# Kernel optimization log

Hardware: AMD Instinct MI355X
Metric: run time of the kernel (lower is better)

The kernel has to match this reference:

```python
import jax, jax.numpy as jnp
import numpy as np

MAX_SEQ_LEN = 1000

def _ln(x, g, b, eps=1e-5):
    m = jnp.mean(x, -1, keepdims=True)
    v = jnp.var(x, -1, keepdims=True)
    return (x - m) * jax.lax.rsqrt(v + eps) * g + b

def _conv1d(x, k, b):
    # x [B,T,Cin], k [K,Cin,Cout], 'SAME' padding (odd kernel)
    return jax.lax.conv_general_dilated(x, k, (1,), 'SAME', dimension_numbers=('NWC', 'WIO', 'NWC')) + b

def _dwconv(x, w):
    # lightweight conv: softmax-normalized depthwise kernel, w [C,K]
    k = jnp.transpose(jax.nn.softmax(w, axis=1))[:, None, :]  # [K,1,C]
    return jax.lax.conv_general_dilated(x, k, (1,), 'SAME', dimension_numbers=('NWC', 'WIO', 'NWC'), feature_group_count=x.shape[-1])

def _conv2d(x, k, b):
    # x [B,H,W,Cin], k [kh,kw,Cin,Cout]
    return jax.lax.conv_general_dilated(x, k, (1, 1), 'SAME', dimension_numbers=('NHWC', 'HWIO', 'NHWC')) + b

def _lconv(x, mask, ln_g, ln_b, glu_w, glu_b, dw, out_w, out_b):
    # LConvBlock: LN -> GLU projection -> depthwise lightweight conv -> out proj -> residual, masked
    res = x
    h = _ln(x, ln_g, ln_b)
    h = h @ glu_w + glu_b
    a, g = jnp.split(h, 2, axis=-1)
    h = a * jax.nn.sigmoid(g)
    h = jnp.where(mask[..., None], 0.0, h)
    h = _dwconv(h, dw)
    h = h @ out_w + out_b
    h = h + res
    return jnp.where(mask[..., None], 0.0, h)

def _forward(content_embedding, speaker_embedding_B, rhythm_B, scaled_duration_outputs,
             in_w, in_b,
             lc0_ln_g, lc0_ln_b, lc0_glu_w, lc0_glu_b, lc0_dw, lc0_out_w, lc0_out_b,
             lc1_ln_g, lc1_ln_b, lc1_glu_w, lc1_glu_b, lc1_dw, lc1_out_w, lc1_out_b,
             p1_w, p1_b, p2_k, p2_b,
             cw_k, cw_b, cw_ln_g, cw_ln_b,
             mkb1_k, mkb1_b, mkb2_k, mkb2_b,
             lw_w, lw_b, ln_g, ln_b, text_mask):
    B, S, _ = content_embedding.shape
    spk = jnp.broadcast_to(speaker_embedding_B[:, None, :], (B, S, speaker_embedding_B.shape[-1]))
    x = jnp.concatenate([content_embedding, spk], -1) @ in_w + in_b
    # duration predictor
    V = _lconv(x, text_mask, lc0_ln_g, lc0_ln_b, lc0_glu_w, lc0_glu_b, lc0_dw, lc0_out_w, lc0_out_b)
    V = _lconv(V, text_mask, lc1_ln_g, lc1_ln_b, lc1_glu_w, lc1_glu_b, lc1_dw, lc1_out_w, lc1_out_b)
    D = jax.nn.softplus(V @ p1_w + p1_b)[..., 0]
    D = jnp.where(text_mask, 0.0, D)
    T = _conv1d(V, p2_k, p2_b)  # [B,S,upsampled_dim]
    # learnable upsampling
    pred_phoneme_len = scaled_duration_outputs.sum(-1)
    alpha_B = jax.lax.stop_gradient(pred_phoneme_len / rhythm_B) / D.sum(-1)
    sD = alpha_B[:, None] * D
    sV = alpha_B[:, None, None] * V
    sT = alpha_B[:, None, None] * T
    mel_len = jnp.clip(jnp.round(sD.sum(-1)).astype(jnp.int32), 1, MAX_SEQ_LEN)
    mel_mask = jnp.arange(MAX_SEQ_LEN)[None, :] >= mel_len[:, None]  # True = pad
    attn_mask = mel_mask[:, :, None] & text_mask[:, None, :]  # bmm(mel_mask, src_mask^T).bool()
    e_k = jnp.cumsum(sD, axis=1)
    s_k = e_k - sD
    t = jnp.arange(1, MAX_SEQ_LEN + 1, dtype=sD.dtype)[None, :, None]
    Sm = jnp.where(attn_mask, 0.0, t - s_k[:, None, :])
    Em = jnp.where(attn_mask, 0.0, e_k[:, None, :] - t)
    # conv_w block: conv1d -> relu -> LN
    Cv = _ln(jax.nn.relu(_conv1d(sV, cw_k, cw_b)), cw_ln_g, cw_ln_b)  # [B,S,CW]
    feat = jnp.concatenate([Sm[..., None], Em[..., None],
                            jnp.broadcast_to(Cv[:, None, :, :], (B, MAX_SEQ_LEN, S, Cv.shape[-1]))], -1)
    h = jax.nn.silu(_conv2d(feat, mkb1_k, mkb1_b))
    h = jax.nn.silu(_conv2d(h, mkb2_k, mkb2_b))
    Wsc = (h @ lw_w + lw_b)[..., 0]  # [B,mel,S]
    Wsc = jnp.where(attn_mask | text_mask[:, None, :], -jnp.inf, Wsc)
    Wmat = jax.nn.softmax(Wsc, axis=2)
    up = jnp.matmul(Wmat, sT)
    up = _ln(up, ln_g, ln_b)
    up = jnp.where(mel_mask[..., None], 0.0, up)
    return up, Wmat, alpha_B, mel_len, mel_mask

def setup_inputs() -> dict:
    key = jax.random.key(0)
    ks = iter(jax.random.split(key, 64))
    B, S, DC, DS, H, CW, MKB, K = 8, 256, 192, 64, 256, 16, 16, 3
    def w(shape, scale=0.02):
        return jax.random.normal(next(ks), shape, jnp.float32) * scale
    inp = {}
    inp['content_embedding'] = jax.random.normal(next(ks), (B, S, DC), jnp.float32)
    inp['speaker_embedding_B'] = jax.random.normal(next(ks), (B, DS), jnp.float32)
    inp['rhythm_B'] = 0.15 + 0.1 * jax.random.uniform(next(ks), (B,), jnp.float32)
    inp['scaled_duration_outputs'] = jax.random.uniform(next(ks), (B, S), jnp.float32)
    lens = jax.random.randint(next(ks), (B,), 200, S + 1)
    inp['text_mask'] = jnp.arange(S)[None, :] >= lens[:, None]
    inp['in_w'] = w((DC + DS, H)); inp['in_b'] = jnp.zeros((H,), jnp.float32)
    for i in range(2):
        inp[f'lc{i}_ln_g'] = jnp.ones((H,), jnp.float32); inp[f'lc{i}_ln_b'] = jnp.zeros((H,), jnp.float32)
        inp[f'lc{i}_glu_w'] = w((H, 2 * H)); inp[f'lc{i}_glu_b'] = jnp.zeros((2 * H,), jnp.float32)
        inp[f'lc{i}_dw'] = w((H, K), 1.0)
        inp[f'lc{i}_out_w'] = w((H, H)); inp[f'lc{i}_out_b'] = jnp.zeros((H,), jnp.float32)
    inp['p1_w'] = w((H, 1)); inp['p1_b'] = jnp.zeros((1,), jnp.float32)
    inp['p2_k'] = w((K, H, H)); inp['p2_b'] = jnp.zeros((H,), jnp.float32)
    inp['cw_k'] = w((K, H, CW)); inp['cw_b'] = jnp.zeros((CW,), jnp.float32)
    inp['cw_ln_g'] = jnp.ones((CW,), jnp.float32); inp['cw_ln_b'] = jnp.zeros((CW,), jnp.float32)
    inp['mkb1_k'] = w((K, K, CW + 2, MKB)); inp['mkb1_b'] = jnp.zeros((MKB,), jnp.float32)
    inp['mkb2_k'] = w((K, K, MKB, MKB)); inp['mkb2_b'] = jnp.zeros((MKB,), jnp.float32)
    inp['lw_w'] = w((MKB, 1)); inp['lw_b'] = jnp.zeros((1,), jnp.float32)
    inp['ln_g'] = jnp.ones((H,), jnp.float32); inp['ln_b'] = jnp.zeros((H,), jnp.float32)
    return inp

def reference(content_embedding, speaker_embedding_B, rhythm_B, scaled_duration_outputs,
              text_mask,
              in_w, in_b,
              lc0_ln_g, lc0_ln_b, lc0_glu_w, lc0_glu_b, lc0_dw, lc0_out_w, lc0_out_b,
              lc1_ln_g, lc1_ln_b, lc1_glu_w, lc1_glu_b, lc1_dw, lc1_out_w, lc1_out_b,
              p1_w, p1_b, p2_k, p2_b,
              cw_k, cw_b, cw_ln_g, cw_ln_b,
              mkb1_k, mkb1_b, mkb2_k, mkb2_b,
              lw_w, lw_b, ln_g, ln_b):
    return _forward(content_embedding, speaker_embedding_B, rhythm_B, scaled_duration_outputs,
                    in_w, in_b,
                    lc0_ln_g, lc0_ln_b, lc0_glu_w, lc0_glu_b, lc0_dw, lc0_out_w, lc0_out_b,
                    lc1_ln_g, lc1_ln_b, lc1_glu_w, lc1_glu_b, lc1_dw, lc1_out_w, lc1_out_b,
                    p1_w, p1_b, p2_k, p2_b,
                    cw_k, cw_b, cw_ln_g, cw_ln_b,
                    mkb1_k, mkb1_b, mkb2_k, mkb2_b,
                    lw_w, lw_b, ln_g, ln_b, text_mask)
```

## Files before the change

### kernel.cpp

```cpp
#include <hip/hip_runtime.h>
#include <math.h>

#define SS 256
#define HH 256
#define MLEN 1000
#define CWW 16
#define NOC 16
#define RB 24

typedef __attribute__((ext_vector_type(8))) short bfrag;
typedef __attribute__((ext_vector_type(4))) float ffrag;

#define WS_X      0u
#define WS_V1     524288u
#define WS_V2     1048576u
#define WS_HB     1572864u
#define WS_STT    1835008u
#define WS_WB     2097152u
#define WS_CCV    2424832u
#define WS_SSV    2457600u
#define WS_CCI    2490368u
#define WS_SSI    2523136u
#define WS_CP     2555904u
#define WS_CV     2654208u
#define WS_EK     2686976u
#define WS_SK     2689024u
#define WS_ALPHA  2691072u
#define WS_MELI   2691080u
#define WS_TMASK  2691088u

#define PK_IN     0u
#define PK_GLU0   65536u
#define PK_GLU1   196608u
#define PK_OUT0   327680u
#define PK_OUT1   393216u
#define PK_P2     458752u

#define OUT_UP    0u
#define OUT_W     2048000u
#define OUT_ALPHA 4096000u
#define OUT_MLEN  4096008u
#define OUT_MMASK 4096016u

__device__ __forceinline__ unsigned bf16rne(float x){
  unsigned u=__float_as_uint(x);
  u += 0x7fffu + ((u>>16)&1u);
  return u;
}
__device__ __forceinline__ unsigned short bf16h(float x){ return (unsigned short)(bf16rne(x)>>16); }
__device__ __forceinline__ float bf2f(unsigned short u){ return __uint_as_float(((unsigned)u)<<16); }
__device__ __forceinline__ unsigned frag_idx(int k,int n,int KT){
  return (unsigned)(((((n>>4)*KT+(k>>5))*64 + ((k>>3)&3)*16 + (n&15))<<3) + (k&7));
}

__global__ __launch_bounds__(256) void k_mask(const void* __restrict__ traw, float* __restrict__ ws){
  __shared__ int s_fu, s_ff, s_nz;
  const unsigned char* mb=(const unsigned char*)traw;
  const unsigned int*  mw=(const unsigned int*)traw;
  int tid=threadIdx.x;
  if(tid==0){s_fu=0;s_ff=0;s_nz=0;}
  __syncthreads();
  int fu=0,ff=0,nz=0;
  for(int w=tid;w<512;w+=256){
    unsigned int v=mw[w];
    if(v){ nz=1; if(v==0x3F800000u) ff=1; else if(v&0xFFFFFF00u) fu=1; }
  }
  if(fu) atomicOr(&s_fu,1);
  if(ff) atomicOr(&s_ff,1);
  if(nz) atomicOr(&s_nz,1);
  __syncthreads();
  int words = (s_ff || (!s_fu && s_nz));
  for(int i=tid;i<2048;i+=256){
    unsigned int v = words ? mw[i] : (unsigned int)mb[i];
    ws[WS_TMASK+i] = v ? 1.0f : 0.0f;
  }
}

__global__ __launch_bounds__(256) void k_prep(const float* __restrict__ in_w,
    const float* __restrict__ g0, const float* __restrict__ g1,
    const float* __restrict__ o0, const float* __restrict__ o1,
    const float* __restrict__ p2k, float* __restrict__ ws){
  unsigned short* wb=(unsigned short*)(ws+WS_WB);
  int gid=blockIdx.x*256+threadIdx.x, stride=gridDim.x*256;
  for(int i=gid;i<65536;i+=stride){ int k=i>>8,n=i&255; wb[PK_IN  +frag_idx(k,n,8)]=bf16h(in_w[i]); }
  for(int i=gid;i<131072;i+=stride){ int k=i>>9,n=i&511; wb[PK_GLU0+frag_idx(k,n,8)]=bf16h(g0[i]); }
  for(int i=gid;i<131072;i+=stride){ int k=i>>9,n=i&511; wb[PK_GLU1+frag_idx(k,n,8)]=bf16h(g1[i]); }
  for(int i=gid;i<65536;i+=stride){ int k=i>>8,n=i&255; wb[PK_OUT0+frag_idx(k,n,8)]=bf16h(o0[i]); }
  for(int i=gid;i<65536;i+=stride){ int k=i>>8,n=i&255; wb[PK_OUT1+frag_idx(k,n,8)]=bf16h(o1[i]); }
  for(int i=gid;i<196608;i+=stride){ int k3=i>>16,r=i&65535,k=r>>8,n=r&255;
    wb[PK_P2+(unsigned)k3*65536u+frag_idx(k,n,8)]=bf16h(p2k[i]); }
}

__global__ __launch_bounds__(256) void k_inproj2(const float* __restrict__ ce, const float* __restrict__ spk,
    const unsigned short* __restrict__ wb, const float* __restrict__ in_b, float* __restrict__ ws){
  __shared__ unsigned short Abf[16][264];
  int m0=(blockIdx.x>>1)*16, nh=blockIdx.x&1, tid=threadIdx.x, b=m0>>8;
  for(int it=0;it<16;it++){
    int m=m0+it;
    float v=(tid<192)? ce[m*192+tid] : spk[b*64+tid-192];
    Abf[it][tid]=bf16h(v);
  }
  __syncthreads();
  int w=tid>>6, lane=tid&63, lq=lane>>4, lm=lane&15;
  ffrag acc[2];
  #pragma unroll
  for(int tt=0;tt<2;tt++){ acc[tt][0]=0.f;acc[tt][1]=0.f;acc[tt][2]=0.f;acc[tt][3]=0.f; }
  #pragma unroll
  for(int kt=0;kt<8;kt++){
    bfrag af=*(const bfrag*)&Abf[lm][kt*32+lq*8];
    #pragma unroll
    for(int tt=0;tt<2;tt++){
      int nt=nh*8+w*2+tt;
      bfrag bf=*(const bfrag*)(wb+((((unsigned)(nt*8+kt))*64u+(unsigned)lane)<<3));
      acc[tt]=__builtin_amdgcn_mfma_f32_16x16x32_bf16(af,bf,acc[tt],0,0,0);
    }
  }
  #pragma unroll
  for(int tt=0;tt<2;tt++){
    int n=nh*128+w*32+tt*16+lm;
    float bn=in_b[n];
    #pragma unroll
    for(int reg=0;reg<4;reg++)
      ws[WS_X+(unsigned)(m0+lq*4+reg)*256u+n]=acc[tt][reg]+bn;
  }
}

__global__ __launch_bounds__(256) void k_glu2(const float* __restrict__ xin,
    const unsigned short* __restrict__ wb, const float* __restrict__ glu_b,
    const float* __restrict__ lgam, const float* __restrict__ lbet,
    const float* __restrict__ tmask, unsigned short* __restrict__ hout){
  __shared__ float Xf[16][264];
  __shared__ unsigned short Abf[16][264];
  __shared__ float gb[2][256];
  __shared__ float tmL[16];
  int m0=(blockIdx.x>>1)*16, nh=blockIdx.x&1, tid=threadIdx.x;
  gb[0][tid]=lgam[tid]; gb[1][tid]=lbet[tid];
  if(tid<16) tmL[tid]=tmask[m0+tid];
  for(int it=0;it<16;it++) Xf[it][tid]=xin[(unsigned)(m0+it)*256u+tid];
  __syncthreads();
  int r=tid>>4, seg=tid&15;
  float s=0.f,q=0.f;
  #pragma unroll
  for(int j4=0;j4<4;j4++){
    float4 v=*(const float4*)&Xf[r][seg*16+j4*4];
    s+=v.x+v.y+v.z+v.w; q+=v.x*v.x+v.y*v.y+v.z*v.z+v.w*v.w;
  }
  s+=__shfl_xor(s,1); q+=__shfl_xor(q,1);
  s+=__shfl_xor(s,2); q+=__shfl_xor(q,2);
  s+=__shfl_xor(s,4); q+=__shfl_xor(q,4);
  s+=__shfl_xor(s,8); q+=__shfl_xor(q,8);
  float mean=s*(1.0f/256.0f), rstd=rsqrtf(q*(1.0f/256.0f)-mean*mean+1e-5f);
  #pragma unroll
  for(int j4=0;j4<4;j4++){
    int c=seg*16+j4*4;
    float4 v=*(const float4*)&Xf[r][c];
    unsigned short o0=bf16h((v.x-mean)*rstd*gb[0][c+0]+gb[1][c+0]);
    unsigned short o1=bf16h((v.y-mean)*rstd*gb[0][c+1]+gb[1][c+1]);
    unsigned short o2=bf16h((v.z-mean)*rstd*gb[0][c+2]+gb[1][c+2]);
    unsigned short o3=bf16h((v.w-mean)*rstd*gb[0][c+3]+gb[1][c+3]);
    *(uint2*)&Abf[r][c]=make_uint2((unsigned)o0|((unsigned)o1<<16),(unsigned)o2|((unsigned)o3<<16));
  }
  __syncthreads();
  int w=tid>>6, lane=tid&63, lq=lane>>4, lm=lane&15;
  ffrag aca[2], acg[2];
  #pragma unroll
  for(int tt=0;tt<2;tt++){ aca[tt][0]=0;aca[tt][1]=0;aca[tt][2]=0;aca[tt][3]=0;
                           acg[tt][0]=0;acg[tt][1]=0;acg[tt][2]=0;acg[tt][3]=0; }
  #pragma unroll
  for(int kt=0;kt<8;kt++){
    bfrag af=*(const bfrag*)&Abf[lm][kt*32+lq*8];
    #pragma unroll
    for(int tt=0;tt<2;tt++){
      int nta=nh*8+w*2+tt, ntg=nta+16;
      bfrag bfa=*(const bfrag*)(wb+((((unsigned)(nta*8+kt))*64u+(unsigned)lane)<<3));
      bfrag bfg=*(const bfrag*)(wb+((((unsigned)(ntg*8+kt))*64u+(unsigned)lane)<<3));
      aca[tt]=__builtin_amdgcn_mfma_f32_16x16x32_bf16(af,bfa,aca[tt],0,0,0);
      acg[tt]=__builtin_amdgcn_mfma_f32_16x16x32_bf16(af,bfg,acg[tt],0,0,0);
    }
  }
  #pragma unroll
  for(int tt=0;tt<2;tt++){
    int n=nh*128+w*32+tt*16+lm;
    float ba=glu_b[n], bg=glu_b[n+256];
    #pragma unroll
    for(int reg=0;reg<4;reg++){
      int row=lq*4+reg;
      float a=aca[tt][reg]+ba, g=acg[tt][reg]+bg;
      float hv=a*(1.0f/(1.0f+__expf(-g)));
      if(tmL[row]!=0.0f) hv=0.0f;
      hout[(unsigned)(m0+row)*256u+n]=bf16h(hv);
    }
  }
}

__global__ __launch_bounds__(256) void k_dwout2(const unsigned short* __restrict__ hb,
    const float* __restrict__ resid, const unsigned short* __restrict__ wb,
    const float* __restrict__ dw, const float* __restrict__ out_b,
    const float* __restrict__ tmask, float* __restrict__ vout){
  __shared__ unsigned short Hb[18][264];
  __shared__ unsigned short Abf[16][264];
  __shared__ float dws[3][256];
  __shared__ float tmL[16];
  int m0=(blockIdx.x>>1)*16, nh=blockIdx.x&1, tid=threadIdx.x, b=m0>>8, s0=m0&255;
  for(int it=0;it<18;it++){
    int sI=s0-1+it;
    Hb[it][tid]=(sI>=0&&sI<256)? hb[(unsigned)(b*256+sI)*256u+tid] : (unsigned short)0;
  }
  {
    float d0=dw[tid*3],d1=dw[tid*3+1],d2=dw[tid*3+2];
    float mx=fmaxf(d0,fmaxf(d1,d2));
    float e0=expf(d0-mx),e1=expf(d1-mx),e2=expf(d2-mx);
    float inv=1.0f/(e0+e1+e2);
    dws[0][tid]=e0*inv; dws[1][tid]=e1*inv; dws[2][tid]=e2*inv;
  }
  if(tid<16) tmL[tid]=tmask[m0+tid];
  __syncthreads();
  float w0=dws[0][tid],w1=dws[1][tid],w2=dws[2][tid];
  for(int it=0;it<16;it++){
    float a=w0*bf2f(Hb[it][tid])+w1*bf2f(Hb[it+1][tid])+w2*bf2f(Hb[it+2][tid]);
    Abf[it][tid]=bf16h(a);
  }
  __syncthreads();
  int w=tid>>6, lane=tid&63, lq=lane>>4, lm=lane&15;
  ffrag acc[2];
  #pragma unroll
  for(int tt=0;tt<2;tt++){ acc[tt][0]=0;acc[tt][1]=0;acc[tt][2]=0;acc[tt][3]=0; }
  #pragma unroll
  for(int kt=0;kt<8;kt++){
    bfrag af=*(const bfrag*)&Abf[lm][kt*32+lq*8];
    #pragma unroll
    for(int tt=0;tt<2;tt++){
      int nt=nh*8+w*2+tt;
      bfrag bf=*(const bfrag*)(wb+((((unsigned)(nt*8+kt))*64u+(unsigned)lane)<<3));
      acc[tt]=__builtin_amdgcn_mfma_f32_16x16x32_bf16(af,bf,acc[tt],0,0,0);
    }
  }
  #pragma unroll
  for(int tt=0;tt<2;tt++){
    int n=nh*128+w*32+tt*16+lm;
    float bn=out_b[n];
    #pragma unroll
    for(int reg=0;reg<4;reg++){
      int row=lq*4+reg, m=m0+row;
      float v=acc[tt][reg]+bn+resid[(unsigned)m*256u+n];
      vout[(unsigned)m*256u+n]=(tmL[row]!=0.0f)?0.0f:v;
    }
  }
}

__global__ __launch_bounds__(256) void k_dur(const float* __restrict__ V2, const float* __restrict__ p1w,
    const float* __restrict__ p1b, const float* __restrict__ sdo, const float* __restrict__ rhythm,
    float* __restrict__ ws, float* __restrict__ outp){
  __shared__ float p1[HH];
  __shared__ float sd[SS];
  __shared__ float red[16];
  int b=blockIdx.x, tid=threadIdx.x;
  int wid=tid>>6, lane=tid&63;
  p1[tid]=p1w[tid];
  __syncthreads();
  float accd=p1b[0];
  const float* row=V2+(unsigned)(b*SS+tid)*HH;
  for(int k=0;k<HH;k+=4){
    float4 v=*(const float4*)&row[k];
    accd+=v.x*p1[k]+v.y*p1[k+1]+v.z*p1[k+2]+v.w*p1[k+3];
  }
  float Dv=fmaxf(accd,0.0f)+log1pf(expf(-fabsf(accd)));
  if(ws[WS_TMASK+b*SS+tid]!=0.0f) Dv=0.0f;
  float sv=sdo[b*SS+tid];
  float a=Dv, c=sv;
  for(int off=32;off;off>>=1){ a+=__shfl_down(a,off); c+=__shfl_down(c,off); }
  if(lane==0){ red[wid]=a; red[wid+8]=c; }
  __syncthreads();
  float Dsum=red[0]+red[1]+red[2]+red[3];
  float pred=red[8]+red[9]+red[10]+red[11];
  float al=(pred/rhythm[b])/Dsum;
  float sDv=al*Dv;
  sd[tid]=sDv;
  __syncthreads();
  for(int off=1;off<SS;off<<=1){
    float t=(tid>=off)?sd[tid-off]:0.0f;
    __syncthreads();
    sd[tid]+=t;
    __syncthreads();
  }
  float ek=sd[tid], sk=ek-sDv;
  ws[WS_EK+b*SS+tid]=ek;
  ws[WS_SK+b*SS+tid]=sk;
  float melf=sd[SS-1];
  int mel=(int)rintf(melf); mel=mel<1?1:(mel>MLEN?MLEN:mel);
  if(tid==0){
    ws[WS_ALPHA+b]=al;
    ((int*)ws)[WS_MELI+b]=mel;
    outp[OUT_ALPHA+b]=al;
    outp[OUT_MLEN+b]=(float)mel;
  }
  for(int t=tid;t<MLEN;t+=SS) outp[OUT_MMASK+b*MLEN+t]=(t>=mel)?1.0f:0.0f;
}

__global__ __launch_bounds__(256) void k_T2(const float* __restrict__ V2,
    const unsigned short* __restrict__ wb, const float* __restrict__ p2b, float* __restrict__ ws){
  __shared__ unsigned short Abf[18][264];
  int m0=(blockIdx.x>>1)*16, nh=blockIdx.x&1, tid=threadIdx.x, b=m0>>8, s0=m0&255;
  for(int it=0;it<18;it++){
    int sI=s0-1+it;
    float v=(sI>=0&&sI<256)? V2[(unsigned)(b*256+sI)*256u+tid] : 0.0f;
    Abf[it][tid]=bf16h(v);
  }
  __syncthreads();
  int w=tid>>6, lane=tid&63, lq=lane>>4, lm=lane&15;
  ffrag acc[2];
  #pragma unroll
  for(int tt=0;tt<2;tt++){ acc[tt][0]=0;acc[tt][1]=0;acc[tt][2]=0;acc[tt][3]=0; }
  for(int k3=0;k3<3;k3++){
    const unsigned short* wb3=wb+(unsigned)k3*65536u;
    #pragma unroll
    for(int kt=0;kt<8;kt++){
      bfrag af=*(const bfrag*)&Abf[lm+k3][kt*32+lq*8];
      #pragma unroll
      for(int tt=0;tt<2;tt++){
        int nt=nh*8+w*2+tt;
        bfrag bf=*(const bfrag*)(wb3+((((unsigned)(nt*8+kt))*64u+(unsigned)lane)<<3));
        acc[tt]=__builtin_amdgcn_mfma_f32_16x16x32_bf16(af,bf,acc[tt],0,0,0);
      }
    }
  }
  float al=ws[WS_ALPHA+b];
  unsigned short* stt=(unsigned short*)(ws+WS_STT);
  #pragma unroll
  for(int tt=0;tt<2;tt++){
    int n=nh*128+w*32+tt*16+lm;
    float bn=p2b[n];
    unsigned short o0=bf16h((acc[tt][0]+bn)*al);
    unsigned short o1=bf16h((acc[tt][1]+bn)*al);
    unsigned short o2=bf16h((acc[tt][2]+bn)*al);
    unsigned short o3=bf16h((acc[tt][3]+bn)*al);
    *(uint2*)&stt[((unsigned)(b*256+n)<<8)+(unsigned)(s0+lq*4)]=
      make_uint2((unsigned)o0|((unsigned)o1<<16),(unsigned)o2|((unsigned)o3<<16));
  }
}

__global__ __launch_bounds__(256) void k_cv(const float* __restrict__ V2, const float* __restrict__ cwk,
    const float* __restrict__ cwb, const float* __restrict__ cwg, const float* __restrict__ cwbe,
    float* __restrict__ ws){
  __shared__ float Vt[18][SS];
  int b=blockIdx.x>>4, tile=blockIdx.x&15, tid=threadIdx.x;
  int sbase=tile*16;
  float al=ws[WS_ALPHA+b];
  for(int rr=0;rr<18;rr++){
    int s=sbase-1+rr;
    Vt[rr][tid]=(s>=0&&s<SS)?al*V2[(b*SS+s)*HH+tid]:0.0f;
  }
  __syncthreads();
  int sl=tid>>4, oc=tid&15;
  float a0=cwb[oc],a1=0.f,a2=0.f,a3=0.f;
  for(int k3=0;k3<3;k3++){
    const float* vp=&Vt[sl+k3][0];
    const float* wpp=cwk+(unsigned)k3*HH*CWW+oc;
    for(int c=0;c<HH;c+=4){
      a0+=vp[c+0]*wpp[(c+0)*CWW];
      a1+=vp[c+1]*wpp[(c+1)*CWW];
      a2+=vp[c+2]*wpp[(c+2)*CWW];
      a3+=vp[c+3]*wpp[(c+3)*CWW];
    }
  }
  float acc=fmaxf((a0+a1)+(a2+a3),0.0f);
  float ssum=acc, qsum=acc*acc;
  for(int off=8;off;off>>=1){ ssum+=__shfl_xor(ssum,off); qsum+=__shfl_xor(qsum,off); }
  float mean=ssum*(1.0f/CWW), var=qsum*(1.0f/CWW)-mean*mean;
  float cv=(acc-mean)*rsqrtf(var+1e-5f)*cwg[oc]+cwbe[oc];
  ws[WS_CV+(unsigned)(b*SS+sbase+sl)*CWW+oc]=cv;
}

__global__ __launch_bounds__(256) void k_cp(const float* __restrict__ mkb1k, const float* __restrict__ mkb1b,
    float* __restrict__ ws){
  __shared__ float CvL[258][17];
  __shared__ float k1c[3][3][CWW][NOC];
  __shared__ float kab[3][3][2][NOC];
  __shared__ float skE[258], ekE[258], fiE[258];
  int b=blockIdx.x, tid=threadIdx.x;
  for(int i=tid;i<3*3*CWW*NOC;i+=256){
    int oc=i&15, ic=(i>>4)&15, kk=i>>8;
    int kw=kk%3, kh=kk/3;
    k1c[kh][kw][ic][oc]=mkb1k[((kh*3+kw)*18+2+ic)*NOC+oc];
  }
  for(int i=tid;i<3*3*2*NOC;i+=256){
    int oc=i&15, ch=(i>>4)&1, kk=i>>5;
    int kw=kk%3, kh=kk/3;
    kab[kh][kw][ch][oc]=mkb1k[((kh*3+kw)*18+ch)*NOC+oc];
  }
  for(int i=tid;i<SS*CWW;i+=256) CvL[1+(i>>4)][i&15]=ws[WS_CV+(unsigned)b*SS*CWW+i];
  if(tid<CWW){ CvL[0][tid]=0.f; CvL[257][tid]=0.f; }
  if(tid<258){
    float sk=0.f, ek=0.f, fi=0.f;
    if(tid>=1 && tid<=SS){
      sk=ws[WS_SK+b*SS+tid-1];
      ek=ws[WS_EK+b*SS+tid-1];
      fi=(ws[WS_TMASK+b*SS+tid-1]!=0.0f)?0.0f:1.0f;
    }
    skE[tid]=sk; ekE[tid]=ek; fiE[tid]=fi;
  }
  __syncthreads();
  float* cpg=ws+WS_CP+(unsigned)b*3*SS*NOC;
  float ccv[16],ssv[16],cci[16],ssi[16];
  #pragma unroll
  for(int oc=0;oc<NOC;oc++){ float bb=mkb1b[oc]; ccv[oc]=bb; cci[oc]=bb; ssv[oc]=0.f; ssi[oc]=0.f; }
  for(int dt=0;dt<3;dt++){
    float acc[NOC];
    #pragma unroll
    for(int oc=0;oc<NOC;oc++) acc[oc]=0.f;
    #pragma unroll
    for(int ds=0;ds<3;ds++){
      #pragma unroll
      for(int ic=0;ic<CWW;ic++){
        float v=CvL[tid+ds][ic];
        #pragma unroll
        for(int oc=0;oc<NOC;oc++) acc[oc]+=v*k1c[dt][ds][ic][oc];
      }
    }
    for(int oc=0;oc<NOC;oc++) cpg[(unsigned)(dt*SS+tid)*NOC+oc]=acc[oc];
    float va[16],vb[16],ia[16],ib2[16];
    #pragma unroll
    for(int oc=0;oc<NOC;oc++){ va[oc]=0.f; vb[oc]=0.f; ia[oc]=0.f; ib2[oc]=0.f; }
    #pragma unroll
    for(int ds=0;ds<3;ds++){
      int j=tid+ds;
      float inb=(j>=1&&j<=SS)?1.0f:0.0f;
      float fb=fiE[j];
      float skv=skE[j], ekv=ekE[j];
      #pragma unroll
      for(int oc=0;oc<NOC;oc++){
        float ka=kab[dt][ds][0][oc], kb=kab[dt][ds][1][oc];
        float d=ka-kb, e=kb*ekv-ka*skv;
        va[oc]+=inb*d; vb[oc]+=inb*e; ia[oc]+=fb*d; ib2[oc]+=fb*e;
      }
    }
    float dtf=(float)dt;
    #pragma unroll
    for(int oc=0;oc<NOC;oc++){
      ccv[oc]+=acc[oc]+vb[oc]+dtf*va[oc]; ssv[oc]+=va[oc];
      cci[oc]+=acc[oc]+ib2[oc]+dtf*ia[oc]; ssi[oc]+=ia[oc];
    }
  }
  unsigned base=(unsigned)(b*SS+tid)*16u;
  for(int oc=0;oc<NOC;oc++){
    ws[WS_CCV+base+oc]=ccv[oc];
    ws[WS_SSV+base+oc]=ssv[oc];
    ws[WS_CCI+base+oc]=cci[oc];
    ws[WS_SSI+base+oc]=ssi[oc];
  }
}

__global__ __launch_bounds__(256,3) void k_stageB(
    const float* __restrict__ ws, const float* __restrict__ mkb1k, const float* __restrict__ mkb1b,
    const float* __restrict__ mkb2k, const float* __restrict__ mkb2b,
    const float* __restrict__ lww, const float* __restrict__ lwb,
    float* __restrict__ outp){
  __shared__ short ringh[3][258][RB];
  __shared__ float skL[258], ekL[258], finL[258];
  __shared__ float wscL[SS];
  __shared__ float red[16];
  int bx=blockIdx.x, b=bx/125, chunk=bx%125, t0=chunk*8, tid=threadIdx.x;
  int wid=tid>>6, lane=tid&63;
  int lq=lane>>4, lm=lane&15;
  if(tid<258){
    float sk=0.f, ek=0.f, fin=0.f;
    if(tid>=1 && tid<=SS){
      sk=ws[WS_SK+b*SS+tid-1];
      ek=ws[WS_EK+b*SS+tid-1];
      fin=(ws[WS_TMASK+b*SS+tid-1]!=0.0f)?0.0f:1.0f;
    }
    skL[tid]=sk; ekL[tid]=ek; finL[tid]=fin;
  }
  if(tid<72){
    int sl=tid/24, rem=tid%24;
    int row=(rem<12)?0:257, c=(rem%12)*2;
    *(int*)&ringh[sl][row][c]=0;
  }
  int mel=((const int*)ws)[WS_MELI+b];
  __syncthreads();

  const float* cpb=ws+WS_CP+(unsigned)b*3*SS*NOC;

  unsigned offA[5]; int dtL[5], zgL[5];
  bfrag bfw[5];
  {
    #pragma unroll
    for(int i=0;i<5;i++){
      int g=4*i+lq;
      int dt,ds,hf,zg;
      if(g<18){ dt=g/6; int rm=g-6*dt; ds=rm>>1; hf=rm&1; zg=0; }
      else { dt=0; ds=0; hf=0; zg=1; }
      int srow=wid*64+lm+ds;
      offA[i]=(unsigned)((srow*RB+8*hf)*2);
      dtL[i]=dt; zgL[i]=zg;
      int pk[4];
      if(!zg){
        #pragma unroll
        for(int j=0;j<4;j++){
          unsigned u0=bf16rne(mkb2k[(8*g+2*j)*NOC+lm]);
          unsigned u1=bf16rne(mkb2k[(8*g+2*j+1)*NOC+lm]);
          pk[j]=(int)((u0>>16)|(u1&0xffff0000u));
        }
      } else pk[0]=pk[1]=pk[2]=pk[3]=0;
      bfw[i]=__builtin_bit_cast(bfrag, make_int4(pk[0],pk[1],pk[2],pk[3]));
    }
  }
  float b2v=mkb2b[lm];
  float lwwv=lww[lm];
  float lwb0=lwb[0];
  const char* ringB=(const char*)&ringh[0][0][0];
  bfrag azero={};

  auto conv1row=[&](int T){
    int s=tid;
    float acc[NOC];
    bool fv=(T>=1)&&(T<=998)&&(T+1<mel);
    bool fi=(T>=2)&&(T<=998)&&(T-1>=mel);
    if(fv||fi){
      const float* cc=ws+(fv?WS_CCV:WS_CCI)+(unsigned)(b*SS+s)*16u;
      const float* s2=ws+(fv?WS_SSV:WS_SSI)+(unsigned)(b*SS+s)*16u;
      float Tf=(float)T;
      #pragma unroll
      for(int q=0;q<4;q++){
        float4 c4=((const float4*)cc)[q];
        float4 s4=((const float4*)s2)[q];
        acc[4*q+0]=c4.x+Tf*s4.x; acc[4*q+1]=c4.y+Tf*s4.y;
        acc[4*q+2]=c4.z+Tf*s4.z; acc[4*q+3]=c4.w+Tf*s4.w;
      }
    } else {
      #pragma unroll
      for(int oc=0;oc<NOC;oc++) acc[oc]=mkb1b[oc];
      #pragma unroll
      for(int dt=0;dt<3;dt++){
        int tr=T+dt-1;
        if(tr<0||tr>=MLEN) continue;
        bool valid=(tr<mel);
        float tt=(float)(tr+1);
        float gg[3], hh[3];
        #pragma unroll
        for(int ds=0;ds<3;ds++){
          int j=s+ds;
          float f = valid ? ((j>=1&&j<=SS)?1.0f:0.0f) : finL[j];
          gg[ds]=f*(tt-skL[j]);
          hh[ds]=f*(ekL[j]-tt);
        }
        const float* cpr=cpb+(unsigned)(dt*SS+s)*NOC;
        float4 c0=((const float4*)cpr)[0], c1=((const float4*)cpr)[1];
        float4 c2=((const float4*)cpr)[2], c3=((const float4*)cpr)[3];
        acc[0]+=c0.x; acc[1]+=c0.y; acc[2]+=c0.z; acc[3]+=c0.w;
        acc[4]+=c1.x; acc[5]+=c1.y; acc[6]+=c1.z; acc[7]+=c1.w;
        acc[8]+=c2.x; acc[9]+=c2.y; acc[10]+=c2.z; acc[11]+=c2.w;
        acc[12]+=c3.x; acc[13]+=c3.y; acc[14]+=c3.z; acc[15]+=c3.w;
        #pragma unroll
        for(int ds=0;ds<3;ds++){
          const float* kA=mkb1k+((dt*3+ds)*18+0)*NOC;
          const float* kB=mkb1k+((dt*3+ds)*18+1)*NOC;
          #pragma unroll
          for(int oc=0;oc<NOC;oc++) acc[oc]+=gg[ds]*kA[oc]+hh[ds]*kB[oc];
        }
      }
    }
    int slot=T%3;
    int pk[8];
    #pragma unroll
    for(int j=0;j<8;j++){
      float x0=acc[2*j], x1=acc[2*j+1];
      float s0=x0/(1.0f+__expf(-x0));
      float s1=x1/(1.0f+__expf(-x1));
      unsigned u0=bf16rne(s0), u1=bf16rne(s1);
      pk[j]=(int)((u0>>16)|(u1&0xffff0000u));
    }
    int4* dst=(int4*)&ringh[slot][s+1][0];
    dst[0]=make_int4(pk[0],pk[1],pk[2],pk[3]);
    dst[1]=make_int4(pk[4],pk[5],pk[6],pk[7]);
  };

  if(t0>0) conv1row(t0-1);
  conv1row(t0);

  #pragma unroll 1
  for(int r=0;r<8;r++){
    int t=t0+r;
    if(t+1<MLEN) conv1row(t+1);
    __syncthreads();
    int tmod=t%3;
    ffrag acc2[4];
    #pragma unroll
    for(int tt=0;tt<4;tt++){ acc2[tt][0]=b2v; acc2[tt][1]=b2v; acc2[tt][2]=b2v; acc2[tt][3]=b2v; }
    #pragma unroll
    for(int i=0;i<5;i++){
      int dt=dtL[i];
      int x=tmod+dt+2; x=(x>=3)?x-3:x; x=(x>=3)?x-3:x;
      int tr=t+dt-1;
      bool av=((unsigned)tr<(unsigned)MLEN)&&(!zgL[i]);
      const char* rp=ringB+(unsigned)x*(258u*RB*2u)+offA[i];
      #pragma unroll
      for(int tt=0;tt<4;tt++){
        int4 ra=*(const int4*)(rp+tt*(16*RB*2));
        bfrag a=av?__builtin_bit_cast(bfrag,ra):azero;
        acc2[tt]=__builtin_amdgcn_mfma_f32_16x16x32_bf16(a,bfw[i],acc2[tt],0,0,0);
      }
    }
    #pragma unroll
    for(int tt=0;tt<4;tt++){
      float out4[4];
      #pragma unroll
      for(int q=0;q<4;q++){
        float xx=acc2[tt][q];
        float pv=(xx/(1.0f+__expf(-xx)))*lwwv;
        pv+=__shfl_xor(pv,1); pv+=__shfl_xor(pv,2); pv+=__shfl_xor(pv,4); pv+=__shfl_xor(pv,8);
        out4[q]=pv+lwb0;
      }
      if(lm==0){
        *(float4*)&wscL[wid*64+tt*16+lq*4]=make_float4(out4[0],out4[1],out4[2],out4[3]);
      }
    }
    __syncthreads();
    float fm=finL[tid+1];
    float wsc=wscL[tid];
    float val=(fm!=0.0f)?wsc:-3.0e38f;
    float mx=val;
    for(int off=32;off;off>>=1) mx=fmaxf(mx,__shfl_down(mx,off));
    if(lane==0) red[wid]=mx;
    __syncthreads();
    mx=fmaxf(fmaxf(red[0],red[1]),fmaxf(red[2],red[3]));
    float e=(fm!=0.0f)?__expf(wsc-mx):0.0f;
    float sm=e;
    for(int off=32;off;off>>=1) sm+=__shfl_down(sm,off);
    if(lane==0) red[8+wid]=sm;
    __syncthreads();
    sm=red[8]+red[9]+red[10]+red[11];
    outp[OUT_W+(unsigned)(b*MLEN+t)*SS+tid]=e/sm;
    __syncthreads();
  }
}

__global__ __launch_bounds__(256) void k_up(const float* __restrict__ ws,
    const float* __restrict__ lng, const float* __restrict__ lnb, float* __restrict__ outp){
  __shared__ unsigned short Wbf[16][264];
  __shared__ float UpL[16][264];
  __shared__ float gb[2][256];
  int bx=blockIdx.x, b=bx/63, tile=bx%63, t0=tile*16, tid=threadIdx.x;
  gb[0][tid]=lng[tid]; gb[1][tid]=lnb[tid];
  for(int it=0;it<16;it++){
    int t=t0+it;
    float v=(t<MLEN)? outp[OUT_W+(unsigned)(b*MLEN+t)*256u+tid] : 0.0f;
    Wbf[it][tid]=bf16h(v);
  }
  int mel=((const int*)ws)[WS_MELI+b];
  __syncthreads();
  int w=tid>>6, lane=tid&63, lq=lane>>4, lm=lane&15;
  const unsigned short* stt=(const unsigned short*)(ws+WS_STT)+(unsigned)b*65536u;
  ffrag acc[4];
  #pragma unroll
  for(int tt=0;tt<4;tt++){ acc[tt][0]=0;acc[tt][1]=0;acc[tt][2]=0;acc[tt][3]=0; }
  #pragma unroll
  for(int kt=0;kt<8;kt++){
    bfrag af=*(const bfrag*)&Wbf[lm][kt*32+lq*8];
    #pragma unroll
    for(int tt=0;tt<4;tt++){
      int n=w*64+tt*16+lm;
      bfrag bf=*(const bfrag*)(stt+((unsigned)n<<8)+(unsigned)(kt*32+lq*8));
      acc[tt]=__builtin_amdgcn_mfma_f32_16x16x32_bf16(af,bf,acc[tt],0,0,0);
    }
  }
  #pragma unroll
  for(int tt=0;tt<4;tt++){
    #pragma unroll
    for(int reg=0;reg<4;reg++)
      UpL[lq*4+reg][w*64+tt*16+lm]=acc[tt][reg];
  }
  __syncthreads();
  int r=tid>>4, seg=tid&15;
  float s=0.f,q=0.f;
  #pragma unroll
  for(int j4=0;j4<4;j4++){
    float4 v=*(const float4*)&UpL[r][seg*16+j4*4];
    s+=v.x+v.y+v.z+v.w; q+=v.x*v.x+v.y*v.y+v.z*v.z+v.w*v.w;
  }
  s+=__shfl_xor(s,1); q+=__shfl_xor(q,1);
  s+=__shfl_xor(s,2); q+=__shfl_xor(q,2);
  s+=__shfl_xor(s,4); q+=__shfl_xor(q,4);
  s+=__shfl_xor(s,8); q+=__shfl_xor(q,8);
  float mean=s*(1.0f/256.0f), rstd=rsqrtf(q*(1.0f/256.0f)-mean*mean+1e-5f);
  int t=t0+r;
  if(t<MLEN){
    bool vld=(t<mel);
    #pragma unroll
    for(int j4=0;j4<4;j4++){
      int c=seg*16+j4*4;
      float4 v=*(const float4*)&UpL[r][c];
      float4 o;
      o.x=vld?((v.x-mean)*rstd*gb[0][c+0]+gb[1][c+0]):0.0f;
      o.y=vld?((v.y-mean)*rstd*gb[0][c+1]+gb[1][c+1]):0.0f;
      o.z=vld?((v.z-mean)*rstd*gb[0][c+2]+gb[1][c+2]):0.0f;
      o.w=vld?((v.w-mean)*rstd*gb[0][c+3]+gb[1][c+3]):0.0f;
      *(float4*)&outp[OUT_UP+(unsigned)(b*MLEN+t)*256u+c]=o;
    }
  }
}

extern "C" void kernel_launch(void* const* d_in, const int* in_sizes, int n_in,
                              void* d_out, int out_size, void* d_ws, size_t ws_size,
                              hipStream_t stream){
  const float* ce   =(const float*)d_in[0];
  const float* spk  =(const float*)d_in[1];
  const float* rhy  =(const float*)d_in[2];
  const float* sdo  =(const float*)d_in[3];
  const void*  tmr  =d_in[4];
  const float* in_w =(const float*)d_in[5];
  const float* in_b =(const float*)d_in[6];
  const float* l0lg =(const float*)d_in[7];
  const float* l0lb =(const float*)d_in[8];
  const float* l0gw =(const float*)d_in[9];
  const float* l0gb =(const float*)d_in[10];
  const float* l0dw =(const float*)d_in[11];
  const float* l0ow =(const float*)d_in[12];
  const float* l0ob =(const float*)d_in[13];
  const float* l1lg =(const float*)d_in[14];
  const float* l1lb =(const float*)d_in[15];
  const float* l1gw =(const float*)d_in[16];
  const float* l1gb =(const float*)d_in[17];
  const float* l1dw =(const float*)d_in[18];
  const float* l1ow =(const float*)d_in[19];
  const float* l1ob =(const float*)d_in[20];
  const float* p1w  =(const float*)d_in[21];
  const float* p1b  =(const float*)d_in[22];
  const float* p2k  =(const float*)d_in[23];
  const float* p2b  =(const float*)d_in[24];
  const float* cwk  =(const float*)d_in[25];
  const float* cwb  =(const float*)d_in[26];
  const float* cwg  =(const float*)d_in[27];
  const float* cwbe =(const float*)d_in[28];
  const float* m1k  =(const float*)d_in[29];
  const float* m1b  =(const float*)d_in[30];
  const float* m2k  =(const float*)d_in[31];
  const float* m2b  =(const float*)d_in[32];
  const float* lww  =(const float*)d_in[33];
  const float* lwbp =(const float*)d_in[34];
  const float* lng  =(const float*)d_in[35];
  const float* lnb  =(const float*)d_in[36];
  float* ws=(float*)d_ws;
  float* outp=(float*)d_out;
  const unsigned short* wbb=(const unsigned short*)(ws+WS_WB);
  unsigned short* hb=(unsigned short*)(ws+WS_HB);

  k_mask   <<<1,256,0,stream>>>(tmr, ws);
  k_prep   <<<256,256,0,stream>>>(in_w, l0gw, l1gw, l0ow, l1ow, p2k, ws);
  k_inproj2<<<256,256,0,stream>>>(ce, spk, wbb+PK_IN, in_b, ws);
  k_glu2   <<<256,256,0,stream>>>(ws+WS_X,  wbb+PK_GLU0, l0gb, l0lg, l0lb, ws+WS_TMASK, hb);
  k_dwout2 <<<256,256,0,stream>>>(hb, ws+WS_X,  wbb+PK_OUT0, l0dw, l0ob, ws+WS_TMASK, ws+WS_V1);
  k_glu2   <<<256,256,0,stream>>>(ws+WS_V1, wbb+PK_GLU1, l1gb, l1lg, l1lb, ws+WS_TMASK, hb);
  k_dwout2 <<<256,256,0,stream>>>(hb, ws+WS_V1, wbb+PK_OUT1, l1dw, l1ob, ws+WS_TMASK, ws+WS_V2);
  k_dur    <<<8,256,0,stream>>>(ws+WS_V2, p1w, p1b, sdo, rhy, ws, outp);
  k_T2     <<<256,256,0,stream>>>(ws+WS_V2, wbb+PK_P2, p2b, ws);
  k_cv     <<<128,256,0,stream>>>(ws+WS_V2, cwk, cwb, cwg, cwbe, ws);
  k_cp     <<<8,256,0,stream>>>(m1k, m1b, ws);
  k_stageB <<<1000,256,0,stream>>>(ws, m1k, m1b, m2k, m2b, lww, lwbp, outp);
  k_up     <<<504,256,0,stream>>>(ws, lng, lnb, outp);
}
```

Before: 328.2 us.

## Fuse front-end LConv pipeline into one halo-tiled kernel and merge post kernels

Merges the mask and weight-prep kernels into one launch. The in-projection, both LConv blocks (LN, GLU, depthwise conv, out-projection, residual) now run in a single kernel per 8-row tile, recomputing a halo of neighbouring rows so intermediates stay in shared memory instead of going through global workspace. T2, cv and cp are folded into one post kernel. stageB stores its mask as bytes and raises the occupancy hint. The aim is fewer launches and less global traffic, paid for with redundant halo rows (8 useful of 16 MFMA rows) and more shared memory per block.

```diff
diff --git a/kernel.cpp b/kernel.cpp
--- a/kernel.cpp
+++ b/kernel.cpp
@@ -11,10 +11,7 @@
 typedef __attribute__((ext_vector_type(8))) short bfrag;
 typedef __attribute__((ext_vector_type(4))) float ffrag;
 
-#define WS_X      0u
-#define WS_V1     524288u
 #define WS_V2     1048576u
-#define WS_HB     1572864u
 #define WS_STT    1835008u
 #define WS_WB     2097152u
 #define WS_CCV    2424832u
@@ -53,35 +50,36 @@
   return (unsigned)(((((n>>4)*KT+(k>>5))*64 + ((k>>3)&3)*16 + (n&15))<<3) + (k&7));
 }
 
-__global__ __launch_bounds__(256) void k_mask(const void* __restrict__ traw, float* __restrict__ ws){
-  __shared__ int s_fu, s_ff, s_nz;
-  const unsigned char* mb=(const unsigned char*)traw;
-  const unsigned int*  mw=(const unsigned int*)traw;
-  int tid=threadIdx.x;
-  if(tid==0){s_fu=0;s_ff=0;s_nz=0;}
-  __syncthreads();
-  int fu=0,ff=0,nz=0;
-  for(int w=tid;w<512;w+=256){
-    unsigned int v=mw[w];
-    if(v){ nz=1; if(v==0x3F800000u) ff=1; else if(v&0xFFFFFF00u) fu=1; }
-  }
-  if(fu) atomicOr(&s_fu,1);
-  if(ff) atomicOr(&s_ff,1);
-  if(nz) atomicOr(&s_nz,1);
-  __syncthreads();
-  int words = (s_ff || (!s_fu && s_nz));
-  for(int i=tid;i<2048;i+=256){
-    unsigned int v = words ? mw[i] : (unsigned int)mb[i];
-    ws[WS_TMASK+i] = v ? 1.0f : 0.0f;
-  }
-}
-
-__global__ __launch_bounds__(256) void k_prep(const float* __restrict__ in_w,
+__global__ __launch_bounds__(256) void k_prepmask(const void* __restrict__ traw,
+    const float* __restrict__ in_w,
     const float* __restrict__ g0, const float* __restrict__ g1,
     const float* __restrict__ o0, const float* __restrict__ o1,
     const float* __restrict__ p2k, float* __restrict__ ws){
+  int tid=threadIdx.x;
+  if(blockIdx.x==256){
+    __shared__ int s_fu, s_ff, s_nz;
+    const unsigned char* mb=(const unsigned char*)traw;
+    const unsigned int*  mw=(const unsigned int*)traw;
+    if(tid==0){s_fu=0;s_ff=0;s_nz=0;}
+    __syncthreads();
+    int fu=0,ff=0,nz=0;
+    for(int w=tid;w<512;w+=256){
+      unsigned int v=mw[w];
+      if(v){ nz=1; if(v==0x3F800000u) ff=1; else if(v&0xFFFFFF00u) fu=1; }
+    }
+    if(fu) atomicOr(&s_fu,1);
+    if(ff) atomicOr(&s_ff,1);
+    if(nz) atomicOr(&s_nz,1);
+    __syncthreads();
+    int words = (s_ff || (!s_fu && s_nz));
+    for(int i=tid;i<2048;i+=256){
+      unsigned int v = words ? mw[i] : (unsigned int)mb[i];
+      ws[WS_TMASK+i] = v ? 1.0f : 0.0f;
+    }
+    return;
+  }
   unsigned short* wb=(unsigned short*)(ws+WS_WB);
-  int gid=blockIdx.x*256+threadIdx.x, stride=gridDim.x*256;
+  int gid=blockIdx.x*256+tid, stride=65536;
   for(int i=gid;i<65536;i+=stride){ int k=i>>8,n=i&255; wb[PK_IN  +frag_idx(k,n,8)]=bf16h(in_w[i]); }
   for(int i=gid;i<131072;i+=stride){ int k=i>>9,n=i&511; wb[PK_GLU0+frag_idx(k,n,8)]=bf16h(g0[i]); }
   for(int i=gid;i<131072;i+=stride){ int k=i>>9,n=i&511; wb[PK_GLU1+frag_idx(k,n,8)]=bf16h(g1[i]); }
@@ -91,159 +89,268 @@
     wb[PK_P2+(unsigned)k3*65536u+frag_idx(k,n,8)]=bf16h(p2k[i]); }
 }
 
-__global__ __launch_bounds__(256) void k_inproj2(const float* __restrict__ ce, const float* __restrict__ spk,
-    const unsigned short* __restrict__ wb, const float* __restrict__ in_b, float* __restrict__ ws){
+__global__ __launch_bounds__(256) void k_front(
+    const float* __restrict__ ce, const float* __restrict__ spk,
+    const unsigned short* __restrict__ wb, const float* __restrict__ in_b,
+    const float* __restrict__ g0b, const float* __restrict__ ln0g, const float* __restrict__ ln0b,
+    const float* __restrict__ dw0, const float* __restrict__ o0b,
+    const float* __restrict__ g1b, const float* __restrict__ ln1g, const float* __restrict__ ln1b,
+    const float* __restrict__ dw1, const float* __restrict__ o1b,
+    const float* __restrict__ tmask, float* __restrict__ V2){
   __shared__ unsigned short Abf[16][264];
-  int m0=(blockIdx.x>>1)*16, nh=blockIdx.x&1, tid=threadIdx.x, b=m0>>8;
+  __shared__ unsigned short Hb[16][264];
+  __shared__ float Xf[16][264];
+  __shared__ float Vf[16][264];
+  __shared__ float dws[2][3][256];
+  __shared__ float tmL[20];
+  int b=blockIdx.x>>5, tile=blockIdx.x&31, s0=tile*8, tid=threadIdx.x;
+  int w=tid>>6, lane=tid&63, lq=lane>>4, lm=lane&15;
+  {
+    float d0=dw0[tid*3],d1=dw0[tid*3+1],d2=dw0[tid*3+2];
+    float mx=fmaxf(d0,fmaxf(d1,d2));
+    float e0=__expf(d0-mx),e1=__expf(d1-mx),e2=__expf(d2-mx);
+    float inv=1.0f/(e0+e1+e2);
+    dws[0][0][tid]=e0*inv; dws[0][1][tid]=e1*inv; dws[0][2][tid]=e2*inv;
+    d0=dw1[tid*3];d1=dw1[tid*3+1];d2=dw1[tid*3+2];
+    mx=fmaxf(d0,fmaxf(d1,d2));
+    e0=__expf(d0-mx);e1=__expf(d1-mx);e2=__expf(d2-mx);
+    inv=1.0f/(e0+e1+e2);
+    dws[1][0][tid]=e0*inv; dws[1][1][tid]=e1*inv; dws[1][2][tid]=e2*inv;
+  }
+  if(tid<18){
+    int sI=s0-2+tid;
+    tmL[tid]=(sI>=0&&sI<256)? tmask[b*256+sI] : 1.0f;
+  }
   for(int it=0;it<16;it++){
-    int m=m0+it;
-    float v=(tid<192)? ce[m*192+tid] : spk[b*64+tid-192];
+    float v=0.f;
+    int sI=s0-2+it;
+    if(it<12 && sI>=0 && sI<256){
+      int m=b*256+sI;
+      v=(tid<192)? ce[m*192+tid] : spk[b*64+tid-192];
+    }
     Abf[it][tid]=bf16h(v);
   }
   __syncthreads();
-  int w=tid>>6, lane=tid&63, lq=lane>>4, lm=lane&15;
-  ffrag acc[2];
-  #pragma unroll
-  for(int tt=0;tt<2;tt++){ acc[tt][0]=0.f;acc[tt][1]=0.f;acc[tt][2]=0.f;acc[tt][3]=0.f; }
-  #pragma unroll
-  for(int kt=0;kt<8;kt++){
-    bfrag af=*(const bfrag*)&Abf[lm][kt*32+lq*8];
-    #pragma unroll
-    for(int tt=0;tt<2;tt++){
-      int nt=nh*8+w*2+tt;
-      bfrag bf=*(const bfrag*)(wb+((((unsigned)(nt*8+kt))*64u+(unsigned)lane)<<3));
-      acc[tt]=__builtin_amdgcn_mfma_f32_16x16x32_bf16(af,bf,acc[tt],0,0,0);
-    }
-  }
-  #pragma unroll
-  for(int tt=0;tt<2;tt++){
-    int n=nh*128+w*32+tt*16+lm;
-    float bn=in_b[n];
-    #pragma unroll
-    for(int reg=0;reg<4;reg++)
-      ws[WS_X+(unsigned)(m0+lq*4+reg)*256u+n]=acc[tt][reg]+bn;
-  }
-}
-
-__global__ __launch_bounds__(256) void k_glu2(const float* __restrict__ xin,
-    const unsigned short* __restrict__ wb, const float* __restrict__ glu_b,
-    const float* __restrict__ lgam, const float* __restrict__ lbet,
-    const float* __restrict__ tmask, unsigned short* __restrict__ hout){
-  __shared__ float Xf[16][264];
-  __shared__ unsigned short Abf[16][264];
-  __shared__ float gb[2][256];
-  __shared__ float tmL[16];
-  int m0=(blockIdx.x>>1)*16, nh=blockIdx.x&1, tid=threadIdx.x;
-  gb[0][tid]=lgam[tid]; gb[1][tid]=lbet[tid];
-  if(tid<16) tmL[tid]=tmask[m0+tid];
-  for(int it=0;it<16;it++) Xf[it][tid]=xin[(unsigned)(m0+it)*256u+tid];
-  __syncthreads();
-  int r=tid>>4, seg=tid&15;
-  float s=0.f,q=0.f;
-  #pragma unroll
-  for(int j4=0;j4<4;j4++){
-    float4 v=*(const float4*)&Xf[r][seg*16+j4*4];
-    s+=v.x+v.y+v.z+v.w; q+=v.x*v.x+v.y*v.y+v.z*v.z+v.w*v.w;
-  }
-  s+=__shfl_xor(s,1); q+=__shfl_xor(q,1);
-  s+=__shfl_xor(s,2); q+=__shfl_xor(q,2);
-  s+=__shfl_xor(s,4); q+=__shfl_xor(q,4);
-  s+=__shfl_xor(s,8); q+=__shfl_xor(q,8);
-  float mean=s*(1.0f/256.0f), rstd=rsqrtf(q*(1.0f/256.0f)-mean*mean+1e-5f);
-  #pragma unroll
-  for(int j4=0;j4<4;j4++){
-    int c=seg*16+j4*4;
-    float4 v=*(const float4*)&Xf[r][c];
-    unsigned short o0=bf16h((v.x-mean)*rstd*gb[0][c+0]+gb[1][c+0]);
-    unsigned short o1=bf16h((v.y-mean)*rstd*gb[0][c+1]+gb[1][c+1]);
-    unsigned short o2=bf16h((v.z-mean)*rstd*gb[0][c+2]+gb[1][c+2]);
-    unsigned short o3=bf16h((v.w-mean)*rstd*gb[0][c+3]+gb[1][c+3]);
-    *(uint2*)&Abf[r][c]=make_uint2((unsigned)o0|((unsigned)o1<<16),(unsigned)o2|((unsigned)o3<<16));
-  }
-  __syncthreads();
-  int w=tid>>6, lane=tid&63, lq=lane>>4, lm=lane&15;
-  ffrag aca[2], acg[2];
-  #pragma unroll
-  for(int tt=0;tt<2;tt++){ aca[tt][0]=0;aca[tt][1]=0;aca[tt][2]=0;aca[tt][3]=0;
-                           acg[tt][0]=0;acg[tt][1]=0;acg[tt][2]=0;acg[tt][3]=0; }
-  #pragma unroll
-  for(int kt=0;kt<8;kt++){
-    bfrag af=*(const bfrag*)&Abf[lm][kt*32+lq*8];
-    #pragma unroll
-    for(int tt=0;tt<2;tt++){
-      int nta=nh*8+w*2+tt, ntg=nta+16;
-      bfrag bfa=*(const bfrag*)(wb+((((unsigned)(nta*8+kt))*64u+(unsigned)lane)<<3));
-      bfrag bfg=*(const bfrag*)(wb+((((unsigned)(ntg*8+kt))*64u+(unsigned)lane)<<3));
-      aca[tt]=__builtin_amdgcn_mfma_f32_16x16x32_bf16(af,bfa,aca[tt],0,0,0);
-      acg[tt]=__builtin_amdgcn_mfma_f32_16x16x32_bf16(af,bfg,acg[tt],0,0,0);
-    }
-  }
-  #pragma unroll
-  for(int tt=0;tt<2;tt++){
-    int n=nh*128+w*32+tt*16+lm;
-    float ba=glu_b[n], bg=glu_b[n+256];
-    #pragma unroll
-    for(int reg=0;reg<4;reg++){
-      int row=lq*4+reg;
-      float a=aca[tt][reg]+ba, g=acg[tt][reg]+bg;
-      float hv=a*(1.0f/(1.0f+__expf(-g)));
-      if(tmL[row]!=0.0f) hv=0.0f;
-      hout[(unsigned)(m0+row)*256u+n]=bf16h(hv);
-    }
-  }
-}
-
-__global__ __launch_bounds__(256) void k_dwout2(const unsigned short* __restrict__ hb,
-    const float* __restrict__ resid, const unsigned short* __restrict__ wb,
-    const float* __restrict__ dw, const float* __restrict__ out_b,
-    const float* __restrict__ tmask, float* __restrict__ vout){
-  __shared__ unsigned short Hb[18][264];
-  __shared__ unsigned short Abf[16][264];
-  __shared__ float dws[3][256];
-  __shared__ float tmL[16];
-  int m0=(blockIdx.x>>1)*16, nh=blockIdx.x&1, tid=threadIdx.x, b=m0>>8, s0=m0&255;
-  for(int it=0;it<18;it++){
-    int sI=s0-1+it;
-    Hb[it][tid]=(sI>=0&&sI<256)? hb[(unsigned)(b*256+sI)*256u+tid] : (unsigned short)0;
-  }
-  {
-    float d0=dw[tid*3],d1=dw[tid*3+1],d2=dw[tid*3+2];
-    float mx=fmaxf(d0,fmaxf(d1,d2));
-    float e0=expf(d0-mx),e1=expf(d1-mx),e2=expf(d2-mx);
-    float inv=1.0f/(e0+e1+e2);
-    dws[0][tid]=e0*inv; dws[1][tid]=e1*inv; dws[2][tid]=e2*inv;
-  }
-  if(tid<16) tmL[tid]=tmask[m0+tid];
-  __syncthreads();
-  float w0=dws[0][tid],w1=dws[1][tid],w2=dws[2][tid];
-  for(int it=0;it<16;it++){
-    float a=w0*bf2f(Hb[it][tid])+w1*bf2f(Hb[it+1][tid])+w2*bf2f(Hb[it+2][tid]);
-    Abf[it][tid]=bf16h(a);
-  }
-  __syncthreads();
-  int w=tid>>6, lane=tid&63, lq=lane>>4, lm=lane&15;
-  ffrag acc[2];
-  #pragma unroll
-  for(int tt=0;tt<2;tt++){ acc[tt][0]=0;acc[tt][1]=0;acc[tt][2]=0;acc[tt][3]=0; }
-  #pragma unroll
-  for(int kt=0;kt<8;kt++){
-    bfrag af=*(const bfrag*)&Abf[lm][kt*32+lq*8];
-    #pragma unroll
-    for(int tt=0;tt<2;tt++){
-      int nt=nh*8+w*2+tt;
-      bfrag bf=*(const bfrag*)(wb+((((unsigned)(nt*8+kt))*64u+(unsigned)lane)<<3));
-      acc[tt]=__builtin_amdgcn_mfma_f32_16x16x32_bf16(af,bf,acc[tt],0,0,0);
-    }
-  }
-  #pragma unroll
-  for(int tt=0;tt<2;tt++){
-    int n=nh*128+w*32+tt*16+lm;
-    float bn=out_b[n];
-    #pragma unroll
-    for(int reg=0;reg<4;reg++){
-      int row=lq*4+reg, m=m0+row;
-      float v=acc[tt][reg]+bn+resid[(unsigned)m*256u+n];
-      vout[(unsigned)m*256u+n]=(tmL[row]!=0.0f)?0.0f:v;
+  {
+    ffrag acc[4];
+    #pragma unroll
+    for(int j=0;j<4;j++){acc[j][0]=0;acc[j][1]=0;acc[j][2]=0;acc[j][3]=0;}
+    #pragma unroll
+    for(int kt=0;kt<8;kt++){
+      bfrag af=*(const bfrag*)&Abf[lm][kt*32+lq*8];
+      #pragma unroll
+      for(int j=0;j<4;j++){
+        int nt=w*4+j;
+        bfrag bf=*(const bfrag*)(wb+PK_IN+((((unsigned)(nt*8+kt))*64u+(unsigned)lane)<<3));
+        acc[j]=__builtin_amdgcn_mfma_f32_16x16x32_bf16(af,bf,acc[j],0,0,0);
+      }
+    }
+    #pragma unroll
+    for(int j=0;j<4;j++){
+      int n=w*64+j*16+lm;
+      float bn=in_b[n];
+      #pragma unroll
+      for(int reg=0;reg<4;reg++) Xf[lq*4+reg][n]=acc[j][reg]+bn;
+    }
+  }
+  __syncthreads();
+  {
+    int r=tid>>4, seg=tid&15;
+    if(r<12){
+      float s=0.f,q=0.f;
+      #pragma unroll
+      for(int j4=0;j4<4;j4++){
+        float4 v=*(const float4*)&Xf[r][seg*16+j4*4];
+        s+=v.x+v.y+v.z+v.w; q+=v.x*v.x+v.y*v.y+v.z*v.z+v.w*v.w;
+      }
+      s+=__shfl_xor(s,1); q+=__shfl_xor(q,1);
+      s+=__shfl_xor(s,2); q+=__shfl_xor(q,2);
+      s+=__shfl_xor(s,4); q+=__shfl_xor(q,4);
+      s+=__shfl_xor(s,8); q+=__shfl_xor(q,8);
+      float mean=s*(1.0f/256.0f), rstd=rsqrtf(q*(1.0f/256.0f)-mean*mean+1e-5f);
+      #pragma unroll
+      for(int j4=0;j4<4;j4++){
+        int c=seg*16+j4*4;
+        float4 v=*(const float4*)&Xf[r][c];
+        unsigned short q0=bf16h((v.x-mean)*rstd*ln0g[c+0]+ln0b[c+0]);
+        unsigned short q1=bf16h((v.y-mean)*rstd*ln0g[c+1]+ln0b[c+1]);
+        unsigned short q2=bf16h((v.z-mean)*rstd*ln0g[c+2]+ln0b[c+2]);
+        unsigned short q3=bf16h((v.w-mean)*rstd*ln0g[c+3]+ln0b[c+3]);
+        *(uint2*)&Abf[r][c]=make_uint2((unsigned)q0|((unsigned)q1<<16),(unsigned)q2|((unsigned)q3<<16));
+      }
+    } else {
+      #pragma unroll
+      for(int j4=0;j4<4;j4++) *(uint2*)&Abf[r][seg*16+j4*4]=make_uint2(0,0);
+    }
+  }
+  __syncthreads();
+  {
+    ffrag aa[4],ag[4];
+    #pragma unroll
+    for(int j=0;j<4;j++){aa[j][0]=0;aa[j][1]=0;aa[j][2]=0;aa[j][3]=0;
+                         ag[j][0]=0;ag[j][1]=0;ag[j][2]=0;ag[j][3]=0;}
+    #pragma unroll
+    for(int kt=0;kt<8;kt++){
+      bfrag af=*(const bfrag*)&Abf[lm][kt*32+lq*8];
+      #pragma unroll
+      for(int j=0;j<4;j++){
+        int nta=w*4+j, ntg=nta+16;
+        bfrag bfa=*(const bfrag*)(wb+PK_GLU0+((((unsigned)(nta*8+kt))*64u+(unsigned)lane)<<3));
+        bfrag bfg=*(const bfrag*)(wb+PK_GLU0+((((unsigned)(ntg*8+kt))*64u+(unsigned)lane)<<3));
+        aa[j]=__builtin_amdgcn_mfma_f32_16x16x32_bf16(af,bfa,aa[j],0,0,0);
+        ag[j]=__builtin_amdgcn_mfma_f32_16x16x32_bf16(af,bfg,ag[j],0,0,0);
+      }
+    }
+    __syncthreads();
+    #pragma unroll
+    for(int j=0;j<4;j++){
+      int n=w*64+j*16+lm;
+      float ba=g0b[n], bg=g0b[n+256];
+      #pragma unroll
+      for(int reg=0;reg<4;reg++){
+        int row=lq*4+reg;
+        float a=aa[j][reg]+ba, g=ag[j][reg]+bg;
+        float hv=a*(1.0f/(1.0f+__expf(-g)));
+        if(row>=12||tmL[row]!=0.0f) hv=0.0f;
+        Hb[row][n]=bf16h(hv);
+      }
+    }
+  }
+  __syncthreads();
+  {
+    float w0=dws[0][0][tid],w1=dws[0][1][tid],w2=dws[0][2][tid];
+    for(int r=0;r<10;r++){
+      float a=w0*bf2f(Hb[r][tid])+w1*bf2f(Hb[r+1][tid])+w2*bf2f(Hb[r+2][tid]);
+      Abf[r][tid]=bf16h(a);
+    }
+    for(int r=10;r<16;r++) Abf[r][tid]=0;
+  }
+  __syncthreads();
+  {
+    ffrag acc[4];
+    #pragma unroll
+    for(int j=0;j<4;j++){acc[j][0]=0;acc[j][1]=0;acc[j][2]=0;acc[j][3]=0;}
+    #pragma unroll
+    for(int kt=0;kt<8;kt++){
+      bfrag af=*(const bfrag*)&Abf[lm][kt*32+lq*8];
+      #pragma unroll
+      for(int j=0;j<4;j++){
+        int nt=w*4+j;
+        bfrag bf=*(const bfrag*)(wb+PK_OUT0+((((unsigned)(nt*8+kt))*64u+(unsigned)lane)<<3));
+        acc[j]=__builtin_amdgcn_mfma_f32_16x16x32_bf16(af,bf,acc[j],0,0,0);
+      }
+    }
+    #pragma unroll
+    for(int j=0;j<4;j++){
+      int n=w*64+j*16+lm;
+      float bn=o0b[n];
+      #pragma unroll
+      for(int reg=0;reg<4;reg++){
+        int row=lq*4+reg;
+        float v=(row<10 && tmL[row+1]==0.0f)? acc[j][reg]+bn+Xf[row+1][n] : 0.0f;
+        Vf[row][n]=v;
+      }
+    }
+  }
+  __syncthreads();
+  {
+    int r=tid>>4, seg=tid&15;
+    if(r<10){
+      float s=0.f,q=0.f;
+      #pragma unroll
+      for(int j4=0;j4<4;j4++){
+        float4 v=*(const float4*)&Vf[r][seg*16+j4*4];
+        s+=v.x+v.y+v.z+v.w; q+=v.x*v.x+v.y*v.y+v.z*v.z+v.w*v.w;
+      }
+      s+=__shfl_xor(s,1); q+=__shfl_xor(q,1);
+      s+=__shfl_xor(s,2); q+=__shfl_xor(q,2);
+      s+=__shfl_xor(s,4); q+=__shfl_xor(q,4);
+      s+=__shfl_xor(s,8); q+=__shfl_xor(q,8);
+      float mean=s*(1.0f/256.0f), rstd=rsqrtf(q*(1.0f/256.0f)-mean*mean+1e-5f);
+      #pragma unroll
+      for(int j4=0;j4<4;j4++){
+        int c=seg*16+j4*4;
+        float4 v=*(const float4*)&Vf[r][c];
+        unsigned short q0=bf16h((v.x-mean)*rstd*ln1g[c+0]+ln1b[c+0]);
+        unsigned short q1=bf16h((v.y-mean)*rstd*ln1g[c+1]+ln1b[c+1]);
+        unsigned short q2=bf16h((v.z-mean)*rstd*ln1g[c+2]+ln1b[c+2]);
+        unsigned short q3=bf16h((v.w-mean)*rstd*ln1g[c+3]+ln1b[c+3]);
+        *(uint2*)&Abf[r][c]=make_uint2((unsigned)q0|((unsigned)q1<<16),(unsigned)q2|((unsigned)q3<<16));
+      }
+    } else {
+      #pragma unroll
+      for(int j4=0;j4<4;j4++) *(uint2*)&Abf[r][seg*16+j4*4]=make_uint2(0,0);
+    }
+  }
+  __syncthreads();
+  {
+    ffrag aa[4],ag[4];
+    #pragma unroll
+    for(int j=0;j<4;j++){aa[j][0]=0;aa[j][1]=0;aa[j][2]=0;aa[j][3]=0;
+                         ag[j][0]=0;ag[j][1]=0;ag[j][2]=0;ag[j][3]=0;}
+    #pragma unroll
+    for(int kt=0;kt<8;kt++){
+      bfrag af=*(const bfrag*)&Abf[lm][kt*32+lq*8];
+      #pragma unroll
+      for(int j=0;j<4;j++){
+        int nta=w*4+j, ntg=nta+16;
+        bfrag bfa=*(const bfrag*)(wb+PK_GLU1+((((unsigned)(nta*8+kt))*64u+(unsigned)lane)<<3));
+        bfrag bfg=*(const bfrag*)(wb+PK_GLU1+((((unsigned)(ntg*8+kt))*64u+(unsigned)lane)<<3));
+        aa[j]=__builtin_amdgcn_mfma_f32_16x16x32_bf16(af,bfa,aa[j],0,0,0);
+        ag[j]=__builtin_amdgcn_mfma_f32_16x16x32_bf16(af,bfg,ag[j],0,0,0);
+      }
+    }
+    __syncthreads();
+    #pragma unroll
+    for(int j=0;j<4;j++){
+      int n=w*64+j*16+lm;
+      float ba=g1b[n], bg=g1b[n+256];
+      #pragma unroll
+      for(int reg=0;reg<4;reg++){
+        int row=lq*4+reg;
+        float a=aa[j][reg]+ba, g=ag[j][reg]+bg;
+        float hv=a*(1.0f/(1.0f+__expf(-g)));
+        if(row>=10||tmL[row+1]!=0.0f) hv=0.0f;
+        Hb[row][n]=bf16h(hv);
+      }
+    }
+  }
+  __syncthreads();
+  {
+    float w0=dws[1][0][tid],w1=dws[1][1][tid],w2=dws[1][2][tid];
+    for(int r=0;r<8;r++){
+      float a=w0*bf2f(Hb[r][tid])+w1*bf2f(Hb[r+1][tid])+w2*bf2f(Hb[r+2][tid]);
+      Abf[r][tid]=bf16h(a);
+    }
+    for(int r=8;r<16;r++) Abf[r][tid]=0;
+  }
+  __syncthreads();
+  {
+    ffrag acc[4];
+    #pragma unroll
+    for(int j=0;j<4;j++){acc[j][0]=0;acc[j][1]=0;acc[j][2]=0;acc[j][3]=0;}
+    #pragma unroll
+    for(int kt=0;kt<8;kt++){
+      bfrag af=*(const bfrag*)&Abf[lm][kt*32+lq*8];
+      #pragma unroll
+      for(int j=0;j<4;j++){
+        int nt=w*4+j;
+        bfrag bf=*(const bfrag*)(wb+PK_OUT1+((((unsigned)(nt*8+kt))*64u+(unsigned)lane)<<3));
+        acc[j]=__builtin_amdgcn_mfma_f32_16x16x32_bf16(af,bf,acc[j],0,0,0);
+      }
+    }
+    #pragma unroll
+    for(int j=0;j<4;j++){
+      int n=w*64+j*16+lm;
+      float bn=o1b[n];
+      #pragma unroll
+      for(int reg=0;reg<4;reg++){
+        int row=lq*4+reg;
+        if(row<8){
+          float v=(tmL[row+2]!=0.0f)? 0.0f : acc[j][reg]+bn+Vf[row+1][n];
+          V2[(unsigned)(b*256+s0+row)*256u+n]=v;
+        }
+      }
     }
   }
 }
@@ -297,179 +404,181 @@
   for(int t=tid;t<MLEN;t+=SS) outp[OUT_MMASK+b*MLEN+t]=(t>=mel)?1.0f:0.0f;
 }
 
-__global__ __launch_bounds__(256) void k_T2(const float* __restrict__ V2,
-    const unsigned short* __restrict__ wb, const float* __restrict__ p2b, float* __restrict__ ws){
-  __shared__ unsigned short Abf[18][264];
-  int m0=(blockIdx.x>>1)*16, nh=blockIdx.x&1, tid=threadIdx.x, b=m0>>8, s0=m0&255;
-  for(int it=0;it<18;it++){
-    int sI=s0-1+it;
-    float v=(sI>=0&&sI<256)? V2[(unsigned)(b*256+sI)*256u+tid] : 0.0f;
-    Abf[it][tid]=bf16h(v);
-  }
-  __syncthreads();
-  int w=tid>>6, lane=tid&63, lq=lane>>4, lm=lane&15;
-  ffrag acc[2];
-  #pragma unroll
-  for(int tt=0;tt<2;tt++){ acc[tt][0]=0;acc[tt][1]=0;acc[tt][2]=0;acc[tt][3]=0; }
-  for(int k3=0;k3<3;k3++){
-    const unsigned short* wb3=wb+(unsigned)k3*65536u;
-    #pragma unroll
-    for(int kt=0;kt<8;kt++){
-      bfrag af=*(const bfrag*)&Abf[lm+k3][kt*32+lq*8];
-      #pragma unroll
-      for(int tt=0;tt<2;tt++){
-        int nt=nh*8+w*2+tt;
-        bfrag bf=*(const bfrag*)(wb3+((((unsigned)(nt*8+kt))*64u+(unsigned)lane)<<3));
-        acc[tt]=__builtin_amdgcn_mfma_f32_16x16x32_bf16(af,bf,acc[tt],0,0,0);
-      }
-    }
-  }
-  float al=ws[WS_ALPHA+b];
-  unsigned short* stt=(unsigned short*)(ws+WS_STT);
-  #pragma unroll
-  for(int tt=0;tt<2;tt++){
-    int n=nh*128+w*32+tt*16+lm;
-    float bn=p2b[n];
-    unsigned short o0=bf16h((acc[tt][0]+bn)*al);
-    unsigned short o1=bf16h((acc[tt][1]+bn)*al);
-    unsigned short o2=bf16h((acc[tt][2]+bn)*al);
-    unsigned short o3=bf16h((acc[tt][3]+bn)*al);
-    *(uint2*)&stt[((unsigned)(b*256+n)<<8)+(unsigned)(s0+lq*4)]=
-      make_uint2((unsigned)o0|((unsigned)o1<<16),(unsigned)o2|((unsigned)o3<<16));
+__global__ __launch_bounds__(256) void k_post(const float* __restrict__ V2,
+    const unsigned short* __restrict__ wbp2, const float* __restrict__ p2b,
+    const float* __restrict__ cwk, const float* __restrict__ cwb,
+    const float* __restrict__ cwg, const float* __restrict__ cwbe,
+    const float* __restrict__ mkb1k, const float* __restrict__ mkb1b,
+    float* __restrict__ ws){
+  int bx=blockIdx.x, tid=threadIdx.x;
+  if(bx<256){
+    __shared__ unsigned short Abf[18][264];
+    int m0=(bx>>1)*16, nh=bx&1, b=m0>>8, s0=m0&255;
+    for(int it=0;it<18;it++){
+      int sI=s0-1+it;
+      float v=(sI>=0&&sI<256)? V2[(unsigned)(b*256+sI)*256u+tid] : 0.0f;
+      Abf[it][tid]=bf16h(v);
+    }
+    __syncthreads();
+    int w=tid>>6, lane=tid&63, lq=lane>>4, lm=lane&15;
+    ffrag acc[2];
+    #pragma unroll
+    for(int tt=0;tt<2;tt++){ acc[tt][0]=0;acc[tt][1]=0;acc[tt][2]=0;acc[tt][3]=0; }
+    for(int k3=0;k3<3;k3++){
+      const unsigned short* wb3=wbp2+(unsigned)k3*65536u;
+      #pragma unroll
+      for(int kt=0;kt<8;kt++){
+        bfrag af=*(const bfrag*)&Abf[lm+k3][kt*32+lq*8];
+        #pragma unroll
+        for(int tt=0;tt<2;tt++){
+          int nt=nh*8+w*2+tt;
+          bfrag bf=*(const bfrag*)(wb3+((((unsigned)(nt*8+kt))*64u+(unsigned)lane)<<3));
+          acc[tt]=__builtin_amdgcn_mfma_f32_16x16x32_bf16(af,bf,acc[tt],0,0,0);
+        }
+      }
+    }
+    float al=ws[WS_ALPHA+b];
+    unsigned short* stt=(unsigned short*)(ws+WS_STT);
+    #pragma unroll
+    for(int tt=0;tt<2;tt++){
+      int n=nh*128+w*32+tt*16+lm;
+      float bn=p2b[n];
+      unsigned short o0=bf16h((acc[tt][0]+bn)*al);
+      unsigned short o1=bf16h((acc[tt][1]+bn)*al);
+      unsigned short o2=bf16h((acc[tt][2]+bn)*al);
+      unsigned short o3=bf16h((acc[tt][3]+bn)*al);
+      *(uint2*)&stt[((unsigned)(b*256+n)<<8)+(unsigned)(s0+lq*4)]=
+        make_uint2((unsigned)o0|((unsigned)o1<<16),(unsigned)o2|((unsigned)o3<<16));
+    }
+  } else if(bx<384){
+    __shared__ float Vt[18][SS];
+    int bb=bx-256;
+    int b=bb>>4, tile=bb&15;
+    int sbase=tile*16;
+    float al=ws[WS_ALPHA+b];
+    for(int rr=0;rr<18;rr++){
+      int s=sbase-1+rr;
+      Vt[rr][tid]=(s>=0&&s<SS)?al*V2[(b*SS+s)*HH+tid]:0.0f;
+    }
+    __syncthreads();
+    int sl=tid>>4, oc=tid&15;
+    float a0=cwb[oc],a1=0.f,a2=0.f,a3=0.f;
+    for(int k3=0;k3<3;k3++){
+      const float* vp=&Vt[sl+k3][0];
+      const float* wpp=cwk+(unsigned)k3*HH*CWW+oc;
+      for(int c=0;c<HH;c+=4){
+        a0+=vp[c+0]*wpp[(c+0)*CWW];
+        a1+=vp[c+1]*wpp[(c+1)*CWW];
+        a2+=vp[c+2]*wpp[(c+2)*CWW];
+        a3+=vp[c+3]*wpp[(c+3)*CWW];
+      }
+    }
+    float acc=fmaxf((a0+a1)+(a2+a3),0.0f);
+    float ssum=acc, qsum=acc*acc;
+    for(int off=8;off;off>>=1){ ssum+=__shfl_xor(ssum,off); qsum+=__shfl_xor(qsum,off); }
+    float mean=ssum*(1.0f/CWW), var=qsum*(1.0f/CWW)-mean*mean;
+    float cv=(acc-mean)*rsqrtf(var+1e-5f)*cwg[oc]+cwbe[oc];
+    ws[WS_CV+(unsigned)(b*SS+sbase+sl)*CWW+oc]=cv;
+  } else {
+    __shared__ float CvL[258][17];
+    __shared__ float k1c[3][3][CWW][NOC];
+    __shared__ float kab[3][3][2][NOC];
+    __shared__ float skE[258], ekE[258], fiE[258];
+    int b=bx-384;
+    for(int i=tid;i<3*3*CWW*NOC;i+=256){
+      int oc=i&15, ic=(i>>4)&15, kk=i>>8;
+      int kw=kk%3, kh=kk/3;
+      k1c[kh][kw][ic][oc]=mkb1k[((kh*3+kw)*18+2+ic)*NOC+oc];
+    }
+    for(int i=tid;i<3*3*2*NOC;i+=256){
+      int oc=i&15, ch=(i>>4)&1, kk=i>>5;
+      int kw=kk%3, kh=kk/3;
+      kab[kh][kw][ch][oc]=mkb1k[((kh*3+kw)*18+ch)*NOC+oc];
+    }
+    for(int i=tid;i<SS*CWW;i+=256) CvL[1+(i>>4)][i&15]=ws[WS_CV+(unsigned)b*SS*CWW+i];
+    if(tid<CWW){ CvL[0][tid]=0.f; CvL[257][tid]=0.f; }
+    if(tid<258){
+      float sk=0.f, ek=0.f, fi=0.f;
+      if(tid>=1 && tid<=SS){
+        sk=ws[WS_SK+b*SS+tid-1];
+        ek=ws[WS_EK+b*SS+tid-1];
+        fi=(ws[WS_TMASK+b*SS+tid-1]!=0.0f)?0.0f:1.0f;
+      }
+      skE[tid]=sk; ekE[tid]=ek; fiE[tid]=fi;
+    }
+    __syncthreads();
+    float* cpg=ws+WS_CP+(unsigned)b*3*SS*NOC;
+    float ccv[16],ssv[16],cci[16],ssi[16];
+    #pragma unroll
+    for(int oc=0;oc<NOC;oc++){ float bb2=mkb1b[oc]; ccv[oc]=bb2; cci[oc]=bb2; ssv[oc]=0.f; ssi[oc]=0.f; }
+    for(int dt=0;dt<3;dt++){
+      float acc[NOC];
+      #pragma unroll
+      for(int oc=0;oc<NOC;oc++) acc[oc]=0.f;
+      #pragma unroll
+      for(int ds=0;ds<3;ds++){
+        #pragma unroll
+        for(int ic=0;ic<CWW;ic++){
+          float v=CvL[tid+ds][ic];
+          #pragma unroll
+          for(int oc=0;oc<NOC;oc++) acc[oc]+=v*k1c[dt][ds][ic][oc];
+        }
+      }
+      for(int oc=0;oc<NOC;oc++) cpg[(unsigned)(dt*SS+tid)*NOC+oc]=acc[oc];
+      float va[16],vb[16],ia[16],ib2[16];
+      #pragma unroll
+      for(int oc=0;oc<NOC;oc++){ va[oc]=0.f; vb[oc]=0.f; ia[oc]=0.f; ib2[oc]=0.f; }
+      #pragma unroll
+      for(int ds=0;ds<3;ds++){
+        int j=tid+ds;
+        float inb=(j>=1&&j<=SS)?1.0f:0.0f;
+        float fb=fiE[j];
+        float skv=skE[j], ekv=ekE[j];
+        #pragma unroll
+        for(int oc=0;oc<NOC;oc++){
+          float ka=kab[dt][ds][0][oc], kb=kab[dt][ds][1][oc];
+          float d=ka-kb, e=kb*ekv-ka*skv;
+          va[oc]+=inb*d; vb[oc]+=inb*e; ia[oc]+=fb*d; ib2[oc]+=fb*e;
+        }
+      }
+      float dtf=(float)dt;
+      #pragma unroll
+      for(int oc=0;oc<NOC;oc++){
+        ccv[oc]+=acc[oc]+vb[oc]+dtf*va[oc]; ssv[oc]+=va[oc];
+        cci[oc]+=acc[oc]+ib2[oc]+dtf*ia[oc]; ssi[oc]+=ia[oc];
+      }
+    }
+    unsigned base=(unsigned)(b*SS+tid)*16u;
+    for(int oc=0;oc<NOC;oc++){
+      ws[WS_CCV+base+oc]=ccv[oc];
+      ws[WS_SSV+base+oc]=ssv[oc];
+      ws[WS_CCI+base+oc]=cci[oc];
+      ws[WS_SSI+base+oc]=ssi[oc];
+    }
   }
 }
 
-__global__ __launch_bounds__(256) void k_cv(const float* __restrict__ V2, const float* __restrict__ cwk,
-    const float* __restrict__ cwb, const float* __restrict__ cwg, const float* __restrict__ cwbe,
-    float* __restrict__ ws){
-  __shared__ float Vt[18][SS];
-  int b=blockIdx.x>>4, tile=blockIdx.x&15, tid=threadIdx.x;
-  int sbase=tile*16;
-  float al=ws[WS_ALPHA+b];
-  for(int rr=0;rr<18;rr++){
-    int s=sbase-1+rr;
-    Vt[rr][tid]=(s>=0&&s<SS)?al*V2[(b*SS+s)*HH+tid]:0.0f;
-  }
-  __syncthreads();
-  int sl=tid>>4, oc=tid&15;
-  float a0=cwb[oc],a1=0.f,a2=0.f,a3=0.f;
-  for(int k3=0;k3<3;k3++){
-    const float* vp=&Vt[sl+k3][0];
-    const float* wpp=cwk+(unsigned)k3*HH*CWW+oc;
-    for(int c=0;c<HH;c+=4){
-      a0+=vp[c+0]*wpp[(c+0)*CWW];
-      a1+=vp[c+1]*wpp[(c+1)*CWW];
-      a2+=vp[c+2]*wpp[(c+2)*CWW];
-      a3+=vp[c+3]*wpp[(c+3)*CWW];
-    }
-  }
-  float acc=fmaxf((a0+a1)+(a2+a3),0.0f);
-  float ssum=acc, qsum=acc*acc;
-  for(int off=8;off;off>>=1){ ssum+=__shfl_xor(ssum,off); qsum+=__shfl_xor(qsum,off); }
-  float mean=ssum*(1.0f/CWW), var=qsum*(1.0f/CWW)-mean*mean;
-  float cv=(acc-mean)*rsqrtf(var+1e-5f)*cwg[oc]+cwbe[oc];
-  ws[WS_CV+(unsigned)(b*SS+sbase+sl)*CWW+oc]=cv;
-}
-
-__global__ __launch_bounds__(256) void k_cp(const float* __restrict__ mkb1k, const float* __restrict__ mkb1b,
-    float* __restrict__ ws){
-  __shared__ float CvL[258][17];
-  __shared__ float k1c[3][3][CWW][NOC];
-  __shared__ float kab[3][3][2][NOC];
-  __shared__ float skE[258], ekE[258], fiE[258];
-  int b=blockIdx.x, tid=threadIdx.x;
-  for(int i=tid;i<3*3*CWW*NOC;i+=256){
-    int oc=i&15, ic=(i>>4)&15, kk=i>>8;
-    int kw=kk%3, kh=kk/3;
-    k1c[kh][kw][ic][oc]=mkb1k[((kh*3+kw)*18+2+ic)*NOC+oc];
-  }
-  for(int i=tid;i<3*3*2*NOC;i+=256){
-    int oc=i&15, ch=(i>>4)&1, kk=i>>5;
-    int kw=kk%3, kh=kk/3;
-    kab[kh][kw][ch][oc]=mkb1k[((kh*3+kw)*18+ch)*NOC+oc];
-  }
-  for(int i=tid;i<SS*CWW;i+=256) CvL[1+(i>>4)][i&15]=ws[WS_CV+(unsigned)b*SS*CWW+i];
-  if(tid<CWW){ CvL[0][tid]=0.f; CvL[257][tid]=0.f; }
-  if(tid<258){
-    float sk=0.f, ek=0.f, fi=0.f;
-    if(tid>=1 && tid<=SS){
-      sk=ws[WS_SK+b*SS+tid-1];
-      ek=ws[WS_EK+b*SS+tid-1];
-      fi=(ws[WS_TMASK+b*SS+tid-1]!=0.0f)?0.0f:1.0f;
-    }
-    skE[tid]=sk; ekE[tid]=ek; fiE[tid]=fi;
-  }
-  __syncthreads();
-  float* cpg=ws+WS_CP+(unsigned)b*3*SS*NOC;
-  float ccv[16],ssv[16],cci[16],ssi[16];
-  #pragma unroll
-  for(int oc=0;oc<NOC;oc++){ float bb=mkb1b[oc]; ccv[oc]=bb; cci[oc]=bb; ssv[oc]=0.f; ssi[oc]=0.f; }
-  for(int dt=0;dt<3;dt++){
-    float acc[NOC];
-    #pragma unroll
-    for(int oc=0;oc<NOC;oc++) acc[oc]=0.f;
-    #pragma unroll
-    for(int ds=0;ds<3;ds++){
-      #pragma unroll
-      for(int ic=0;ic<CWW;ic++){
-        float v=CvL[tid+ds][ic];
-        #pragma unroll
-        for(int oc=0;oc<NOC;oc++) acc[oc]+=v*k1c[dt][ds][ic][oc];
-      }
-    }
-    for(int oc=0;oc<NOC;oc++) cpg[(unsigned)(dt*SS+tid)*NOC+oc]=acc[oc];
-    float va[16],vb[16],ia[16],ib2[16];
-    #pragma unroll
-    for(int oc=0;oc<NOC;oc++){ va[oc]=0.f; vb[oc]=0.f; ia[oc]=0.f; ib2[oc]=0.f; }
-    #pragma unroll
-    for(int ds=0;ds<3;ds++){
-      int j=tid+ds;
-      float inb=(j>=1&&j<=SS)?1.0f:0.0f;
-      float fb=fiE[j];
-      float skv=skE[j], ekv=ekE[j];
-      #pragma unroll
-      for(int oc=0;oc<NOC;oc++){
-        float ka=kab[dt][ds][0][oc], kb=kab[dt][ds][1][oc];
-        float d=ka-kb, e=kb*ekv-ka*skv;
-        va[oc]+=inb*d; vb[oc]+=inb*e; ia[oc]+=fb*d; ib2[oc]+=fb*e;
-      }
-    }
-    float dtf=(float)dt;
-    #pragma unroll
-    for(int oc=0;oc<NOC;oc++){
-      ccv[oc]+=acc[oc]+vb[oc]+dtf*va[oc]; ssv[oc]+=va[oc];
-      cci[oc]+=acc[oc]+ib2[oc]+dtf*ia[oc]; ssi[oc]+=ia[oc];
-    }
-  }
-  unsigned base=(unsigned)(b*SS+tid)*16u;
-  for(int oc=0;oc<NOC;oc++){
-    ws[WS_CCV+base+oc]=ccv[oc];
-    ws[WS_SSV+base+oc]=ssv[oc];
-    ws[WS_CCI+base+oc]=cci[oc];
-    ws[WS_SSI+base+oc]=ssi[oc];
-  }
-}
-
-__global__ __launch_bounds__(256,3) void k_stageB(
+__global__ __launch_bounds__(256,4) void k_stageB(
     const float* __restrict__ ws, const float* __restrict__ mkb1k, const float* __restrict__ mkb1b,
     const float* __restrict__ mkb2k, const float* __restrict__ mkb2b,
     const float* __restrict__ lww, const float* __restrict__ lwb,
     float* __restrict__ outp){
   __shared__ short ringh[3][258][RB];
-  __shared__ float skL[258], ekL[258], finL[258];
-  __shared__ float wscL[SS];
+  __shared__ float skL[258], ekL[258];
+  __shared__ unsigned char finC[260];
+  __shared__ __align__(16) float wscL[SS];
   __shared__ float red[16];
   int bx=blockIdx.x, b=bx/125, chunk=bx%125, t0=chunk*8, tid=threadIdx.x;
   int wid=tid>>6, lane=tid&63;
   int lq=lane>>4, lm=lane&15;
   if(tid<258){
-    float sk=0.f, ek=0.f, fin=0.f;
+    float sk=0.f, ek=0.f; unsigned char fin=0;
     if(tid>=1 && tid<=SS){
       sk=ws[WS_SK+b*SS+tid-1];
       ek=ws[WS_EK+b*SS+tid-1];
-      fin=(ws[WS_TMASK+b*SS+tid-1]!=0.0f)?0.0f:1.0f;
-    }
-    skL[tid]=sk; ekL[tid]=ek; finL[tid]=fin;
+      fin=(ws[WS_TMASK+b*SS+tid-1]!=0.0f)?0:1;
+    }
+    skL[tid]=sk; ekL[tid]=ek; finC[tid]=fin;
   }
   if(tid<72){
     int sl=tid/24, rem=tid%24;
@@ -540,7 +649,7 @@
         #pragma unroll
         for(int ds=0;ds<3;ds++){
           int j=s+ds;
-          float f = valid ? ((j>=1&&j<=SS)?1.0f:0.0f) : finL[j];
+          float f = valid ? ((j>=1&&j<=SS)?1.0f:0.0f) : (float)finC[j];
           gg[ds]=f*(tt-skL[j]);
           hh[ds]=f*(ekL[j]-tt);
         }
@@ -616,7 +725,7 @@
       }
     }
     __syncthreads();
-    float fm=finL[tid+1];
+    float fm=(float)finC[tid+1];
     float wsc=wscL[tid];
     float val=(fm!=0.0f)?wsc:-3.0e38f;
     float mx=val;
@@ -743,19 +852,14 @@
   float* ws=(float*)d_ws;
   float* outp=(float*)d_out;
   const unsigned short* wbb=(const unsigned short*)(ws+WS_WB);
-  unsigned short* hb=(unsigned short*)(ws+WS_HB);
-
-  k_mask   <<<1,256,0,stream>>>(tmr, ws);
-  k_prep   <<<256,256,0,stream>>>(in_w, l0gw, l1gw, l0ow, l1ow, p2k, ws);
-  k_inproj2<<<256,256,0,stream>>>(ce, spk, wbb+PK_IN, in_b, ws);
-  k_glu2   <<<256,256,0,stream>>>(ws+WS_X,  wbb+PK_GLU0, l0gb, l0lg, l0lb, ws+WS_TMASK, hb);
-  k_dwout2 <<<256,256,0,stream>>>(hb, ws+WS_X,  wbb+PK_OUT0, l0dw, l0ob, ws+WS_TMASK, ws+WS_V1);
-  k_glu2   <<<256,256,0,stream>>>(ws+WS_V1, wbb+PK_GLU1, l1gb, l1lg, l1lb, ws+WS_TMASK, hb);
-  k_dwout2 <<<256,256,0,stream>>>(hb, ws+WS_V1, wbb+PK_OUT1, l1dw, l1ob, ws+WS_TMASK, ws+WS_V2);
-  k_dur    <<<8,256,0,stream>>>(ws+WS_V2, p1w, p1b, sdo, rhy, ws, outp);
-  k_T2     <<<256,256,0,stream>>>(ws+WS_V2, wbb+PK_P2, p2b, ws);
-  k_cv     <<<128,256,0,stream>>>(ws+WS_V2, cwk, cwb, cwg, cwbe, ws);
-  k_cp     <<<8,256,0,stream>>>(m1k, m1b, ws);
-  k_stageB <<<1000,256,0,stream>>>(ws, m1k, m1b, m2k, m2b, lww, lwbp, outp);
-  k_up     <<<504,256,0,stream>>>(ws, lng, lnb, outp);
+
+  k_prepmask<<<257,256,0,stream>>>(tmr, in_w, l0gw, l1gw, l0ow, l1ow, p2k, ws);
+  k_front   <<<256,256,0,stream>>>(ce, spk, wbb, in_b,
+                                   l0gb, l0lg, l0lb, l0dw, l0ob,
+                                   l1gb, l1lg, l1lb, l1dw, l1ob,
+                                   ws+WS_TMASK, ws+WS_V2);
+  k_dur     <<<8,256,0,stream>>>(ws+WS_V2, p1w, p1b, sdo, rhy, ws, outp);
+  k_post    <<<392,256,0,stream>>>(ws+WS_V2, wbb+PK_P2, p2b, cwk, cwb, cwg, cwbe, m1k, m1b, ws);
+  k_stageB  <<<1000,256,0,stream>>>(ws, m1k, m1b, m2k, m2b, lww, lwbp, outp);
+  k_up      <<<504,256,0,stream>>>(ws, lng, lnb, outp);
 }
```

Result: faster. 310.6 us (-5.3%).
